# Kernel tuning notes

Measured on AMD Instinct MI355X. Metric: run time of the kernel, lower is better.

The kernel has to match this reference:

```python
import jax, jax.numpy as jnp
import numpy as np

# Problem sizes
N, E, G = 100000, 400000, 2048      # nodes, edges, graphs
NIN, H, NHID, NOUT = 300, 256, 512, 768
NL, T = 3, 16                        # extra atom GAT layers (num_layers=4), pooling timesteps
SLOPE = 0.01                         # leaky_relu negative slope (PyG AttentiveFP uses 0.01)


def setup_inputs() -> dict:
    ks = iter(jax.random.split(jax.random.key(0), 80))
    def rn(shape, s=0.1):
        return jax.random.normal(next(ks), shape, dtype=jnp.float32) * s
    inp = {
        "x": rn((N, NIN), 1.0),
        "edge_attr": rn((E, 1), 1.0),
        # learned parameters (inference mode: dropout disabled)
        "lin1_W": rn((H, NIN)), "lin1_b": rn((H,)),
        # GATEConv
        "g_lin1_W": rn((H, H + 1)), "g_lin2_W": rn((H, H)),
        "g_att_l": rn((H,)), "g_att_r": rn((H,)), "g_bias": rn((H,)),
        "gru0_wih": rn((3 * H, H)), "gru0_whh": rn((3 * H, H)),
        "gru0_bih": rn((3 * H,)), "gru0_bhh": rn((3 * H,)),
        # 3 atom GATConv layers (stacked)
        "atom_W": rn((NL, H, H)), "atom_att_src": rn((NL, H)),
        "atom_att_dst": rn((NL, H)), "atom_bias": rn((NL, H)),
        "agru_wih": rn((NL, 3 * H, H)), "agru_whh": rn((NL, 3 * H, H)),
        "agru_bih": rn((NL, 3 * H)), "agru_bhh": rn((NL, 3 * H)),
        # molecule-level GATConv + GRU (16 timesteps)
        "mol_W": rn((H, H)), "mol_att_src": rn((H,)),
        "mol_att_dst": rn((H,)), "mol_bias": rn((H,)),
        "mgru_wih": rn((3 * H, H)), "mgru_whh": rn((3 * H, H)),
        "mgru_bih": rn((3 * H,)), "mgru_bhh": rn((3 * H,)),
        "lin2_W": rn((NHID, H)), "lin2_b": rn((NHID,)),
        "fc1_W": rn((NOUT, NHID)), "fc1_b": rn((NOUT,)),
        # int inputs
        "edge_index": jax.random.randint(next(ks), (2, E), 0, N),
        "batch": jnp.sort(jax.random.randint(next(ks), (N,), 0, G)),
    }
    return inp


def _lrelu(x):
    return jnp.where(x >= 0, x, SLOPE * x)


def _gru(xin, h, wih, whh, bih, bhh):
    gi = xin @ wih.T + bih
    gh = h @ whh.T + bhh
    ir, iz, inn = jnp.split(gi, 3, axis=-1)
    hr, hz, hn = jnp.split(gh, 3, axis=-1)
    r = jax.nn.sigmoid(ir + hr)
    z = jax.nn.sigmoid(iz + hz)
    n = jnp.tanh(inn + r * hn)
    return (1.0 - z) * n + z * h


def _seg_softmax(a, idx, n):
    m = jax.ops.segment_max(a, idx, num_segments=n)
    e = jnp.exp(a - m[idx])
    s = jax.ops.segment_sum(e, idx, num_segments=n)
    return e / s[idx]


def reference(x, edge_attr, lin1_W, lin1_b, g_lin1_W, g_lin2_W, g_att_l, g_att_r,
              g_bias, gru0_wih, gru0_whh, gru0_bih, gru0_bhh, atom_W, atom_att_src,
              atom_att_dst, atom_bias, agru_wih, agru_whh, agru_bih, agru_bhh,
              mol_W, mol_att_src, mol_att_dst, mol_bias, mgru_wih, mgru_whh,
              mgru_bih, mgru_bhh, lin2_W, lin2_b, fc1_W, fc1_b, edge_index, batch):
    src, dst = edge_index[0], edge_index[1]
    # input projection
    x = _lrelu(x @ lin1_W.T + lin1_b)                                   # [N, H]
    # GATEConv: edge-feature attention
    ge = _lrelu(jnp.concatenate([x[src], edge_attr], axis=-1) @ g_lin1_W.T)  # [E, H]
    a = _lrelu(ge @ g_att_l + (x @ g_att_r)[dst])                       # [E]
    alpha = _seg_softmax(a, dst, N)
    h = jax.ops.segment_sum((x[src] @ g_lin2_W.T) * alpha[:, None], dst,
                            num_segments=N) + g_bias
    x = jax.nn.relu(_gru(jax.nn.elu(h), x, gru0_wih, gru0_whh, gru0_bih, gru0_bhh))
    # remaining atom GATConv + GRU layers
    for l in range(NL):
        xw = x @ atom_W[l].T                                            # [N, H]
        a = _lrelu((xw @ atom_att_src[l])[src] + (xw @ atom_att_dst[l])[dst])
        alpha = _seg_softmax(a, dst, N)
        h = jax.ops.segment_sum(xw[src] * alpha[:, None], dst,
                                num_segments=N) + atom_bias[l]
        x = jax.nn.relu(_gru(jax.nn.elu(h), x, agru_wih[l], agru_whh[l],
                             agru_bih[l], agru_bhh[l]))
    # attentive global pooling (node -> graph bipartite GAT, 16 timesteps)
    out = jax.nn.relu(jax.ops.segment_sum(x, batch, num_segments=G))    # [G, H]
    xw = x @ mol_W.T                                                    # shared lin for src/dst
    a_src = xw @ mol_att_src                                            # [N]
    for _ in range(T):
        a = _lrelu(a_src + ((out @ mol_W.T) @ mol_att_dst)[batch])      # [N]
        alpha = _seg_softmax(a, batch, G)
        h = jax.ops.segment_sum(xw * alpha[:, None], batch,
                                num_segments=G) + mol_bias
        out = jax.nn.relu(_gru(jax.nn.elu(h), out, mgru_wih, mgru_whh,
                               mgru_bih, mgru_bhh))
    out = out @ lin2_W.T + lin2_b                                       # [G, NHID]
    # encoder head: relu -> (global_mean_pool is identity on graph-level emb) -> fc1
    return jax.nn.relu(out) @ fc1_W.T + fc1_b                           # [G, NOUT]
```

## Files before the change

### kernel.cpp

```cpp
#include <hip/hip_runtime.h>
#include <hip/hip_bf16.h>
#include <hip/hip_fp16.h>
#include <math.h>

typedef __attribute__((ext_vector_type(8))) short           short8;
typedef __attribute__((ext_vector_type(8))) unsigned short  ushort8;
typedef __attribute__((ext_vector_type(4))) unsigned short  us4;
typedef __attribute__((ext_vector_type(4))) float           f32x4;

__device__ __forceinline__ float lreluf(float v){ return v >= 0.f ? v : 0.01f*v; }
__device__ __forceinline__ float sigf(float v){ return 1.f/(1.f + expf(-v)); }

#define OP_NONE  0
#define OP_LRELU 1
#define OP_RELU  2

#define GLDS16(gp, lp) __builtin_amdgcn_global_load_lds( \
    (const __attribute__((address_space(1))) void*)(gp), \
    (__attribute__((address_space(3))) void*)(lp), 16, 0, 0)

__device__ __forceinline__ float applyOp(float v, int op){
  if (op == OP_LRELU) return v >= 0.f ? v : 0.01f*v;
  if (op == OP_RELU)  return v > 0.f ? v : 0.f;
  return v;
}

__device__ __forceinline__ unsigned short f2b(float f){
  unsigned x = __float_as_uint(f);
  unsigned lsb = (x >> 16) & 1u;
  return (unsigned short)((x + 0x7fffu + lsb) >> 16);
}
__device__ __forceinline__ float b2f(unsigned short h){
  return __uint_as_float((unsigned)h << 16);
}
__device__ __forceinline__ void split2(float v, unsigned short& h, unsigned short& l){
  h = f2b(v);
  l = f2b(v - b2f(h));
}
__device__ __forceinline__ float rec2(unsigned short h, unsigned short l){
  return b2f(h) + b2f(l);
}
__device__ __forceinline__ unsigned short f2h(float f){
  return __half_as_ushort(__float2half(f));
}
__device__ __forceinline__ float h2f(unsigned short u){
  return __half2float(__ushort_as_half(u));
}

__device__ __forceinline__ int ldsOff(int row, int chunk){
  return row*32 + ((chunk ^ ((row >> 1) & 3)) << 3);
}

__device__ __forceinline__ float blkSum(float v, float* red){
  int t = threadIdx.x;
  red[t] = v; __syncthreads();
  for (int s = 128; s > 0; s >>= 1){ if (t < s) red[t] += red[t+s]; __syncthreads(); }
  float r = red[0]; __syncthreads();
  return r;
}
__device__ __forceinline__ float blkMax(float v, float* red){
  int t = threadIdx.x;
  red[t] = v; __syncthreads();
  for (int s = 128; s > 0; s >>= 1){ if (t < s) red[t] = fmaxf(red[t], red[t+s]); __syncthreads(); }
  float r = red[0]; __syncthreads();
  return r;
}

__device__ __forceinline__ f32x4 mfma3(short8 aH, short8 aL, short8 bH, short8 bL, f32x4 acc){
  acc = __builtin_amdgcn_mfma_f32_16x16x32_bf16(aL, bH, acc, 0, 0, 0);
  acc = __builtin_amdgcn_mfma_f32_16x16x32_bf16(aH, bL, acc, 0, 0, 0);
  acc = __builtin_amdgcn_mfma_f32_16x16x32_bf16(aH, bH, acc, 0, 0, 0);
  return acc;
}

__global__ void wsplit_k(const float* __restrict__ src, unsigned short* __restrict__ Hd,
                         unsigned short* __restrict__ Ld, int lda, int K, long long tot)
{
  long long i = (long long)blockIdx.x*256 + threadIdx.x;
  if (i >= tot) return;
  long long r = i / K; int c = (int)(i % K);
  float v = src[r*lda + c];
  unsigned short h = f2b(v);
  Hd[r*(long long)K + c] = h;
  Ld[r*(long long)K + c] = f2b(v - b2f(h));
}

__device__ __forceinline__ void stagePS(const unsigned short* __restrict__ GH,
    const unsigned short* __restrict__ GL, int ldk, int row0, int k0,
    unsigned short* __restrict__ ldsH, unsigned short* __restrict__ ldsL, int tid)
{
  int r = tid >> 2;
  int c = (tid & 3) ^ ((r >> 1) & 3);
  size_t go = (size_t)(row0 + r)*ldk + k0 + c*8;
  int wbase = (tid >> 6) * 512;
  GLDS16(&GH[go], &ldsH[wbase]);
  GLDS16(&GL[go], &ldsL[wbase]);
}

__device__ __forceinline__ void stage2(const float* __restrict__ src, int lda,
    int row0, int rowmax, int k0, int K,
    unsigned short* __restrict__ ldsH, unsigned short* __restrict__ ldsL, int tid)
{
  int r = tid >> 2, c = tid & 3;
  int gr = row0 + r, gk = k0 + c*8;
  const float* p = src + (size_t)gr*lda + gk;
  float f[8];
  if (gr < rowmax && gk + 8 <= K && ((lda & 3) == 0)){
    float4 f0 = *(const float4*)p;
    float4 f1 = *(const float4*)(p+4);
    f[0]=f0.x; f[1]=f0.y; f[2]=f0.z; f[3]=f0.w;
    f[4]=f1.x; f[5]=f1.y; f[6]=f1.z; f[7]=f1.w;
  } else {
    #pragma unroll
    for (int j = 0; j < 8; ++j) f[j] = (gr < rowmax && gk + j < K) ? p[j] : 0.f;
  }
  ushort8 vh, vl;
  #pragma unroll
  for (int j = 0; j < 8; ++j){
    unsigned short h, l; split2(f[j], h, l);
    vh[j] = h; vl[j] = l;
  }
  int off = ldsOff(r, c);
  *(ushort8*)&ldsH[off] = vh;
  *(ushort8*)&ldsL[off] = vl;
}

__global__ __launch_bounds__(256) void gemm_mfma_k(
    const float* __restrict__ A, int lda,
    const float* __restrict__ W, int ldw,
    const float* __restrict__ bias,
    unsigned short* __restrict__ CH, unsigned short* __restrict__ CL,
    int M, int N, int K, int op)
{
  __shared__ unsigned short AsH[64*32], AsL[64*32];
  __shared__ unsigned short WsH[64*32], WsL[64*32];
  const int tid = threadIdx.x;
  const int bm = blockIdx.y * 64, bn = blockIdx.x * 64;
  const int wave = tid >> 6, lane = tid & 63;
  const int wr = wave >> 1, wc = wave & 1;
  const int quad = lane >> 4, id = lane & 15;

  f32x4 acc[2][2] = {};
  const int iters = (K + 31) / 32;
  for (int kt = 0; kt < iters; ++kt){
    int k0 = kt * 32;
    stage2(A, lda, bm, M, k0, K, AsH, AsL, tid);
    stage2(W, ldw, bn, N, k0, K, WsH, WsL, tid);
    __syncthreads();
    short8 aH[2], aL[2], bH[2], bL[2];
    #pragma unroll
    for (int i = 0; i < 2; ++i){
      int off = ldsOff(wr*32 + i*16 + id, quad);
      aH[i] = *(const short8*)&AsH[off];
      aL[i] = *(const short8*)&AsL[off];
    }
    #pragma unroll
    for (int j = 0; j < 2; ++j){
      int off = ldsOff(wc*32 + j*16 + id, quad);
      bH[j] = *(const short8*)&WsH[off];
      bL[j] = *(const short8*)&WsL[off];
    }
    #pragma unroll
    for (int i = 0; i < 2; ++i)
      #pragma unroll
      for (int j = 0; j < 2; ++j)
        acc[i][j] = mfma3(aH[i], aL[i], bH[j], bL[j], acc[i][j]);
    __syncthreads();
  }
  #pragma unroll
  for (int i = 0; i < 2; ++i){
    int gr0 = bm + wr*32 + i*16 + quad*4;
    #pragma unroll
    for (int j = 0; j < 2; ++j){
      int gc = bn + wc*32 + j*16 + id;
      if (gc >= N) continue;
      float bv = bias ? bias[gc] : 0.f;
      #pragma unroll
      for (int r = 0; r < 4; ++r){
        int row = gr0 + r;
        if (row >= M) continue;
        float v = applyOp(acc[i][j][r] + bv, op);
        unsigned short h, l; split2(v, h, l);
        CH[(size_t)row*N + gc] = h;
        CL[(size_t)row*N + gc] = l;
      }
    }
  }
}

__global__ __launch_bounds__(256) void gemm_ps_k(
    const unsigned short* __restrict__ AH, const unsigned short* __restrict__ AL,
    const unsigned short* __restrict__ WH_, const unsigned short* __restrict__ WL_,
    const float* __restrict__ bias, float* __restrict__ C,
    unsigned short* __restrict__ CH, unsigned short* __restrict__ CL,
    int M, int N, int K, int op, int ncb)
{
  __shared__ unsigned short AsH[64*32], AsL[64*32];
  __shared__ unsigned short WsH[64*32], WsL[64*32];
  int nwg = gridDim.x, bid = blockIdx.x;
  int q = nwg >> 3, r = nwg & 7;
  int xcd = bid & 7, jj = bid >> 3;
  int idx = (xcd < r ? xcd*(q+1) : r*(q+1) + (xcd - r)*q) + jj;
  const int bm = (idx / ncb)*64, bn = (idx % ncb)*64;
  const int tid = threadIdx.x;
  const int wave = tid >> 6, lane = tid & 63;
  const int wr = wave >> 1, wc = wave & 1;
  const int quad = lane >> 4, id = lane & 15;

  f32x4 acc[2][2] = {};
  const int iters = K >> 5;
  for (int kt = 0; kt < iters; ++kt){
    int k0 = kt * 32;
    stagePS(AH, AL, K, bm, k0, AsH, AsL, tid);
    stagePS(WH_, WL_, K, bn, k0, WsH, WsL, tid);
    __syncthreads();
    short8 aH[2], aL[2], bH[2], bL[2];
    #pragma unroll
    for (int i = 0; i < 2; ++i){
      int off = ldsOff(wr*32 + i*16 + id, quad);
      aH[i] = *(const short8*)&AsH[off];
      aL[i] = *(const short8*)&AsL[off];
    }
    #pragma unroll
    for (int j = 0; j < 2; ++j){
      int off = ldsOff(wc*32 + j*16 + id, quad);
      bH[j] = *(const short8*)&WsH[off];
      bL[j] = *(const short8*)&WsL[off];
    }
    #pragma unroll
    for (int i = 0; i < 2; ++i)
      #pragma unroll
      for (int j = 0; j < 2; ++j)
        acc[i][j] = mfma3(aH[i], aL[i], bH[j], bL[j], acc[i][j]);
    __syncthreads();
  }
  #pragma unroll
  for (int i = 0; i < 2; ++i){
    int gr0 = bm + wr*32 + i*16 + quad*4;
    #pragma unroll
    for (int j = 0; j < 2; ++j){
      int gc = bn + wc*32 + j*16 + id;
      float bv = bias ? bias[gc] : 0.f;
      #pragma unroll
      for (int rr = 0; rr < 4; ++rr){
        int row = gr0 + rr;
        if (row >= M) continue;
        float v = applyOp(acc[i][j][rr] + bv, op);
        if (C)  C[(size_t)row*N + gc] = v;
        if (CH){
          if (CL){
            unsigned short h, l; split2(v, h, l);
            CH[(size_t)row*N + gc] = h;
            CL[(size_t)row*N + gc] = l;
          } else {
            CH[(size_t)row*N + gc] = f2h(v);
          }
        }
      }
    }
  }
}

__global__ __launch_bounds__(256) void gemm2_ps_k(
    const unsigned short* __restrict__ AH, const unsigned short* __restrict__ AL,
    const unsigned short* __restrict__ W1H, const unsigned short* __restrict__ W1L,
    const unsigned short* __restrict__ W2H, const unsigned short* __restrict__ W2L,
    unsigned short* __restrict__ YB, unsigned short* __restrict__ ZB, int M)
{
  __shared__ unsigned short AsH[64*32], AsL[64*32];
  __shared__ unsigned short U1H[64*32], U1L[64*32];
  __shared__ unsigned short U2H[64*32], U2L[64*32];
  int nwg = gridDim.x, bid = blockIdx.x;
  int q = nwg >> 3, r = nwg & 7;
  int xcd = bid & 7, jj = bid >> 3;
  int idx = (xcd < r ? xcd*(q+1) : r*(q+1) + (xcd - r)*q) + jj;
  const int bm = (idx >> 2)*64, bn = (idx & 3)*64;
  const int tid = threadIdx.x;
  const int wave = tid >> 6, lane = tid & 63;
  const int wr = wave >> 1, wc = wave & 1;
  const int quad = lane >> 4, id = lane & 15;

  f32x4 acc1[2][2] = {}, acc2[2][2] = {};
  for (int kt = 0; kt < 8; ++kt){
    int k0 = kt * 32;
    stagePS(AH, AL, 256, bm, k0, AsH, AsL, tid);
    stagePS(W1H, W1L, 256, bn, k0, U1H, U1L, tid);
    stagePS(W2H, W2L, 256, bn, k0, U2H, U2L, tid);
    __syncthreads();
    short8 aH[2], aL[2];
    #pragma unroll
    for (int i = 0; i < 2; ++i){
      int off = ldsOff(wr*32 + i*16 + id, quad);
      aH[i] = *(const short8*)&AsH[off];
      aL[i] = *(const short8*)&AsL[off];
    }
    #pragma unroll
    for (int j = 0; j < 2; ++j){
      int off = ldsOff(wc*32 + j*16 + id, quad);
      short8 bh, bl;
      bh = *(const short8*)&U1H[off]; bl = *(const short8*)&U1L[off];
      #pragma unroll
      for (int i = 0; i < 2; ++i) acc1[i][j] = mfma3(aH[i], aL[i], bh, bl, acc1[i][j]);
      bh = *(const short8*)&U2H[off]; bl = *(const short8*)&U2L[off];
      #pragma unroll
      for (int i = 0; i < 2; ++i) acc2[i][j] = mfma3(aH[i], aL[i], bh, bl, acc2[i][j]);
    }
    __syncthreads();
  }
  #pragma unroll
  for (int i = 0; i < 2; ++i){
    int gr0 = bm + wr*32 + i*16 + quad*4;
    #pragma unroll
    for (int j = 0; j < 2; ++j){
      int gc = bn + wc*32 + j*16 + id;
      #pragma unroll
      for (int rr = 0; rr < 4; ++rr){
        int row = gr0 + rr;
        if (row >= M) continue;
        YB[(size_t)row*256 + gc] = f2h(acc1[i][j][rr]);
        ZB[(size_t)row*256 + gc] = f2h(acc2[i][j][rr]);
      }
    }
  }
}

__device__ __forceinline__ void gru_phase_ps(
    const unsigned short* __restrict__ AH, const unsigned short* __restrict__ AL,
    const unsigned short* __restrict__ WH_, const unsigned short* __restrict__ WL_,
    int bm, int bn, int tid, int wr, int wc, int quad, int id,
    unsigned short* AsH, unsigned short* AsL,
    unsigned short* W0H, unsigned short* W0L,
    unsigned short* W1H, unsigned short* W1L,
    unsigned short* W2H, unsigned short* W2L,
    f32x4 (&accR)[2][2], f32x4 (&accZ)[2][2], f32x4 (&accN)[2][2])
{
  for (int kt = 0; kt < 8; ++kt){
    int k0 = kt * 32;
    stagePS(AH, AL, 256, bm, k0, AsH, AsL, tid);
    stagePS(WH_,          WL_,          256, bn, k0, W0H, W0L, tid);
    stagePS(WH_ + 65536,  WL_ + 65536,  256, bn, k0, W1H, W1L, tid);
    stagePS(WH_ + 131072, WL_ + 131072, 256, bn, k0, W2H, W2L, tid);
    __syncthreads();
    short8 aH[2], aL[2];
    #pragma unroll
    for (int i = 0; i < 2; ++i){
      int off = ldsOff(wr*32 + i*16 + id, quad);
      aH[i] = *(const short8*)&AsH[off];
      aL[i] = *(const short8*)&AsL[off];
    }
    #pragma unroll
    for (int j = 0; j < 2; ++j){
      int off = ldsOff(wc*32 + j*16 + id, quad);
      short8 bh, bl;
      bh = *(const short8*)&W0H[off]; bl = *(const short8*)&W0L[off];
      #pragma unroll
      for (int i = 0; i < 2; ++i) accR[i][j] = mfma3(aH[i], aL[i], bh, bl, accR[i][j]);
      bh = *(const short8*)&W1H[off]; bl = *(const short8*)&W1L[off];
      #pragma unroll
      for (int i = 0; i < 2; ++i) accZ[i][j] = mfma3(aH[i], aL[i], bh, bl, accZ[i][j]);
      bh = *(const short8*)&W2H[off]; bl = *(const short8*)&W2L[off];
      #pragma unroll
      for (int i = 0; i < 2; ++i) accN[i][j] = mfma3(aH[i], aL[i], bh, bl, accN[i][j]);
    }
    __syncthreads();
  }
}

__global__ __launch_bounds__(256) void gru_ps_k(
    const unsigned short* __restrict__ XinH, const unsigned short* __restrict__ XinL,
    const unsigned short* __restrict__ HidH, const unsigned short* __restrict__ HidL,
    const unsigned short* __restrict__ wihH, const unsigned short* __restrict__ wihL,
    const unsigned short* __restrict__ whhH, const unsigned short* __restrict__ whhL,
    const float* __restrict__ bih, const float* __restrict__ bhh,
    unsigned short* __restrict__ OutH, unsigned short* __restrict__ OutL, int M)
{
  __shared__ unsigned short AsH[64*32], AsL[64*32];
  __shared__ unsigned short W0H[64*32], W0L[64*32];
  __shared__ unsigned short W1H[64*32], W1L[64*32];
  __shared__ unsigned short W2H[64*32], W2L[64*32];
  int nwg = gridDim.x, bid = blockIdx.x;
  int q = nwg >> 3, r = nwg & 7;
  int xcd = bid & 7, jj = bid >> 3;
  int idx = (xcd < r ? xcd*(q+1) : r*(q+1) + (xcd - r)*q) + jj;
  const int bm = (idx >> 2)*64, bn = (idx & 3)*64;
  const int tid = threadIdx.x;
  const int wave = tid >> 6, lane = tid & 63;
  const int wr = wave >> 1, wc = wave & 1;
  const int quad = lane >> 4, id = lane & 15;

  f32x4 accR[2][2] = {}, accZ[2][2] = {}, accI[2][2] = {}, accH[2][2] = {};

  gru_phase_ps(XinH, XinL, wihH, wihL, bm, bn, tid, wr, wc, quad, id,
               AsH, AsL, W0H, W0L, W1H, W1L, W2H, W2L, accR, accZ, accI);
  gru_phase_ps(HidH, HidL, whhH, whhL, bm, bn, tid, wr, wc, quad, id,
               AsH, AsL, W0H, W0L, W1H, W1L, W2H, W2L, accR, accZ, accH);

  #pragma unroll
  for (int i = 0; i < 2; ++i){
    int gr0 = bm + wr*32 + i*16 + quad*4;
    #pragma unroll
    for (int j = 0; j < 2; ++j){
      int gc = bn + wc*32 + j*16 + id;
      float br_  = bih[gc]     + bhh[gc];
      float bz_  = bih[256+gc] + bhh[256+gc];
      float bn_i = bih[512+gc], bn_h = bhh[512+gc];
      #pragma unroll
      for (int rr = 0; rr < 4; ++rr){
        int row = gr0 + rr;
        if (row >= M) continue;
        float rg = sigf(accR[i][j][rr] + br_);
        float zg = sigf(accZ[i][j][rr] + bz_);
        float ng = tanhf(accI[i][j][rr] + bn_i + rg*(accH[i][j][rr] + bn_h));
        float hv = rec2(HidH[(size_t)row*256 + gc], HidL[(size_t)row*256 + gc]);
        float o = (1.f - zg)*ng + zg*hv;
        o = o > 0.f ? o : 0.f;
        unsigned short h, l; split2(o, h, l);
        OutH[(size_t)row*256 + gc] = h;
        OutL[(size_t)row*256 + gc] = l;
      }
    }
  }
}

__global__ __launch_bounds__(256) void rowdot2_ps_k(
    const unsigned short* __restrict__ XH, const unsigned short* __restrict__ XL,
    const float* __restrict__ w1, const float* __restrict__ w2,
    float* __restrict__ y1, float* __restrict__ y2, int M)
{
  int m = blockIdx.x*4 + (threadIdx.x >> 6);
  if (m >= M) return;
  int lane = threadIdx.x & 63;
  us4 vh = *(const us4*)&XH[(size_t)m*256 + lane*4];
  us4 vl = *(const us4*)&XL[(size_t)m*256 + lane*4];
  float p1 = 0.f, p2 = 0.f;
  #pragma unroll
  for (int u = 0; u < 4; ++u){
    float xv = rec2(vh[u], vl[u]);
    int c = lane*4 + u;
    p1 += xv * w1[c];
    if (w2) p2 += xv * w2[c];
  }
  for (int o = 32; o > 0; o >>= 1){
    p1 += __shfl_down(p1, o);
    if (w2) p2 += __shfl_down(p2, o);
  }
  if (lane == 0){ y1[m] = p1; if (w2) y2[m] = p2; }
}

__global__ __launch_bounds__(256) void rowdot_b_k(
    const unsigned short* __restrict__ XB,
    const float* __restrict__ w1, const float* __restrict__ w2,
    float* __restrict__ y1, float* __restrict__ y2, int M)
{
  int m = blockIdx.x*4 + (threadIdx.x >> 6);
  if (m >= M) return;
  int lane = threadIdx.x & 63;
  us4 vh = *(const us4*)&XB[(size_t)m*256 + lane*4];
  float p1 = 0.f, p2 = 0.f;
  #pragma unroll
  for (int u = 0; u < 4; ++u){
    float xv = h2f(vh[u]);
    int c = lane*4 + u;
    p1 += xv * w1[c];
    if (w2) p2 += xv * w2[c];
  }
  for (int o = 32; o > 0; o >>= 1){
    p1 += __shfl_down(p1, o);
    if (w2) p2 += __shfl_down(p2, o);
  }
  if (lane == 0){ y1[m] = p1; if (w2) y2[m] = p2; }
}

__global__ void hist_k(const int* __restrict__ key, unsigned* __restrict__ deg, int E){
  int e = blockIdx.x*256 + threadIdx.x;
  if (e >= E) return;
  atomicAdd(&deg[key[e]], 1u);
}

__global__ __launch_bounds__(256) void scan1_k(const unsigned* __restrict__ deg,
    unsigned* __restrict__ incl, unsigned* __restrict__ bsum, int N)
{
  __shared__ unsigned sm[256];
  int t = threadIdx.x;
  int i = blockIdx.x*256 + t;
  unsigned v = (i < N) ? deg[i] : 0u;
  sm[t] = v; __syncthreads();
  for (int s = 1; s < 256; s <<= 1){
    unsigned u = (t >= s) ? sm[t - s] : 0u;
    __syncthreads();
    sm[t] += u;
    __syncthreads();
  }
  if (i < N) incl[i] = sm[t];
  if (t == 255) bsum[blockIdx.x] = sm[255];
}

__global__ __launch_bounds__(256) void scan2_k(unsigned* __restrict__ bsum, int nb){
  __shared__ unsigned sm[256];
  __shared__ unsigned carry;
  int t = threadIdx.x;
  if (t == 0) carry = 0u;
  __syncthreads();
  for (int base = 0; base < nb; base += 256){
    int i = base + t;
    unsigned v = (i < nb) ? bsum[i] : 0u;
    sm[t] = v; __syncthreads();
    for (int s = 1; s < 256; s <<= 1){
      unsigned u = (t >= s) ? sm[t - s] : 0u;
      __syncthreads();
      sm[t] += u;
      __syncthreads();
    }
    unsigned total = sm[255];
    unsigned c = carry;
    if (i < nb) bsum[i] = c + sm[t] - v;
    __syncthreads();
    if (t == 0) carry = c + total;
    __syncthreads();
  }
}

__global__ void scan3_k(const unsigned* __restrict__ incl, const unsigned* __restrict__ deg,
    const unsigned* __restrict__ bsum, unsigned* __restrict__ off, int N, int E)
{
  int i = blockIdx.x*256 + threadIdx.x;
  if (i < N) off[i] = incl[i] - deg[i] + bsum[blockIdx.x];
  if (i == 0) off[N] = (unsigned)E;
}

__global__ void fill_k(const int* __restrict__ src, const int* __restrict__ dst,
    const unsigned* __restrict__ off, unsigned* __restrict__ cur,
    int* __restrict__ csr_src, int* __restrict__ csr_eid, int* __restrict__ epos, int E)
{
  int e = blockIdx.x*256 + threadIdx.x;
  if (e >= E) return;
  int d = dst[e];
  unsigned p = off[d] + atomicAdd(&cur[d], 1u);
  csr_src[p] = src[e];
  csr_eid[p] = e;
  epos[e] = (int)p;
}

__global__ void fill2_k(const int* __restrict__ src, const int* __restrict__ epos,
    const unsigned* __restrict__ off2, unsigned* __restrict__ cur,
    int* __restrict__ csc_pos, int E)
{
  int e = blockIdx.x*256 + threadIdx.x;
  if (e >= E) return;
  int s = src[e];
  unsigned qq = off2[s] + atomicAdd(&cur[s], 1u);
  csc_pos[qq] = epos[e];
}

__global__ __launch_bounds__(256) void gate_edge_score_csc_k(
    const unsigned short* __restrict__ YB,
    const float* __restrict__ g_lin1W,
    const float* __restrict__ att_l, const float* __restrict__ ea_in,
    const float* __restrict__ xr,
    const unsigned* __restrict__ off2, const int* __restrict__ csc_pos,
    const int* __restrict__ csr_eid, const int* __restrict__ dst,
    float* __restrict__ a_out, int N, int H)
{
  int s = blockIdx.x*4 + (threadIdx.x >> 6);
  if (s >= N) return;
  int lane = threadIdx.x & 63;
  unsigned q0 = off2[s], q1 = off2[s+1];
  if (q0 == q1) return;
  us4 vh = *(const us4*)&YB[(size_t)s*256 + lane*4];
  float y4[4], w4[4], a4[4];
  #pragma unroll
  for (int u = 0; u < 4; ++u){
    int c = lane*4 + u;
    y4[u] = h2f(vh[u]);
    w4[u] = g_lin1W[(size_t)c*(H+1) + H];
    a4[u] = att_l[c];
  }
  for (unsigned qq = q0; qq < q1; ++qq){
    int p = csc_pos[qq];
    int e = csr_eid[p];
    int d = dst[e];
    float eav = ea_in[e];
    float acc = 0.f;
    #pragma unroll
    for (int u = 0; u < 4; ++u)
      acc += lreluf(y4[u] + eav * w4[u]) * a4[u];
    for (int o = 32; o > 0; o >>= 1) acc += __shfl_down(acc, o);
    if (lane == 0) a_out[p] = lreluf(acc + xr[d]);
  }
}

__global__ void node_softmax_k(const unsigned* __restrict__ off, const int* __restrict__ csr_src,
    const float* __restrict__ nd1, const float* __restrict__ nd2,
    float* __restrict__ w, int N, int mode)
{
  int n = blockIdx.x*256 + threadIdx.x;
  if (n >= N) return;
  unsigned p0 = off[n], p1 = off[n+1];
  float m = -INFINITY;
  if (mode){
    float d = nd2[n];
    for (unsigned p = p0; p < p1; ++p){
      float a = lreluf(nd1[csr_src[p]] + d);
      w[p] = a;
      m = fmaxf(m, a);
    }
  } else {
    for (unsigned p = p0; p < p1; ++p) m = fmaxf(m, w[p]);
  }
  float ssum = 0.f;
  for (unsigned p = p0; p < p1; ++p){
    float e = expf(w[p] - m);
    w[p] = e; ssum += e;
  }
  float inv = (ssum > 0.f) ? 1.f/ssum : 0.f;
  for (unsigned p = p0; p < p1; ++p) w[p] *= inv;
}

__global__ __launch_bounds__(256) void gather_h_k(
    const unsigned short* __restrict__ ZB,
    const float* __restrict__ w, const unsigned* __restrict__ off,
    const int* __restrict__ csr_src, const float* __restrict__ bias,
    unsigned short* __restrict__ hH, unsigned short* __restrict__ hL, int N)
{
  int n = blockIdx.x*4 + (threadIdx.x >> 6);
  if (n >= N) return;
  int lane = threadIdx.x & 63;
  unsigned p0 = off[n], p1 = off[n+1];
  float4 acc = make_float4(0.f, 0.f, 0.f, 0.f);
  if (p0 < p1){
    us4 zh_n = *(const us4*)&ZB[(size_t)csr_src[p0]*256 + lane*4];
    float w_n = w[p0];
    for (unsigned p = p0; p < p1; ++p){
      us4 zh = zh_n;
      float wv = w_n;
      if (p + 1 < p1){
        zh_n = *(const us4*)&ZB[(size_t)csr_src[p+1]*256 + lane*4];
        w_n = w[p+1];
      }
      acc.x = fmaf(wv, h2f(zh[0]), acc.x);
      acc.y = fmaf(wv, h2f(zh[1]), acc.y);
      acc.z = fmaf(wv, h2f(zh[2]), acc.z);
      acc.w = fmaf(wv, h2f(zh[3]), acc.w);
    }
  }
  const float4 b = *(const float4*)&bias[lane*4];
  float vals[4];
  float v;
  v = acc.x + b.x; vals[0] = v > 0.f ? v : expf(v) - 1.f;
  v = acc.y + b.y; vals[1] = v > 0.f ? v : expf(v) - 1.f;
  v = acc.z + b.z; vals[2] = v > 0.f ? v : expf(v) - 1.f;
  v = acc.w + b.w; vals[3] = v > 0.f ? v : expf(v) - 1.f;
  us4 vh, vl;
  #pragma unroll
  for (int u = 0; u < 4; ++u){
    unsigned short h, l; split2(vals[u], h, l);
    vh[u] = h; vl[u] = l;
  }
  *(us4*)&hH[(size_t)n*256 + lane*4] = vh;
  *(us4*)&hL[(size_t)n*256 + lane*4] = vl;
}

__global__ void seg_bounds_k(const int* __restrict__ batch, unsigned* __restrict__ gs,
                             unsigned* __restrict__ ge, int N){
  int n = blockIdx.x*256 + threadIdx.x;
  if (n >= N) return;
  int g = batch[n];
  atomicMin(&gs[g], (unsigned)n);
  atomicMax(&ge[g], (unsigned)(n+1));
}
__global__ __launch_bounds__(256) void graph_pool_k(
    const unsigned short* __restrict__ xH, const unsigned short* __restrict__ xL,
    const unsigned* __restrict__ gs, const unsigned* __restrict__ ge,
    unsigned short* __restrict__ outgH, unsigned short* __restrict__ outgL)
{
  int g = blockIdx.x, t = threadIdx.x;
  unsigned s0 = gs[g], e0 = ge[g];
  float acc = 0.f;
  for (unsigned n = s0; n < e0; ++n)
    acc += rec2(xH[(size_t)n*256 + t], xL[(size_t)n*256 + t]);
  acc = acc > 0.f ? acc : 0.f;
  unsigned short h, l; split2(acc, h, l);
  outgH[(size_t)g*256 + t] = h;
  outgL[(size_t)g*256 + t] = l;
}
__global__ void precompute_v_k(const float* __restrict__ W, const float* __restrict__ ad,
                               float* __restrict__ v){
  int i = threadIdx.x;
  float acc = 0.f;
  for (int j = 0; j < 256; ++j) acc += W[(size_t)j*256 + i] * ad[j];
  v[i] = acc;
}
__global__ __launch_bounds__(256) void mol_pool_k(
    const unsigned short* __restrict__ ogH, const unsigned short* __restrict__ ogL,
    const float* __restrict__ v, const float* __restrict__ asrc,
    const unsigned short* __restrict__ xwB,
    const unsigned* __restrict__ gs, const unsigned* __restrict__ geb,
    const float* __restrict__ bias,
    unsigned short* __restrict__ hgH, unsigned short* __restrict__ hgL)
{
  __shared__ float red[256];
  int g = blockIdx.x, t = threadIdx.x;
  float ogv = rec2(ogH[(size_t)g*256 + t], ogL[(size_t)g*256 + t]);
  float tg = blkSum(ogv * v[t], red);
  unsigned s0 = gs[g], e0 = geb[g];
  float mx = -INFINITY;
  for (unsigned n = s0 + t; n < e0; n += 256) mx = fmaxf(mx, lreluf(asrc[n] + tg));
  mx = blkMax(mx, red);
  float sm = 0.f;
  for (unsigned n = s0 + t; n < e0; n += 256) sm += expf(lreluf(asrc[n] + tg) - mx);
  sm = blkSum(sm, red);
  float acc = 0.f;
  if (e0 > s0 && sm > 0.f){
    float inv = 1.f / sm;
    for (unsigned n = s0; n < e0; ++n){
      float w = expf(lreluf(asrc[n] + tg) - mx) * inv;
      acc = fmaf(w, h2f(xwB[(size_t)n*256 + t]), acc);
    }
  }
  float h0 = acc + bias[t];
  h0 = h0 > 0.f ? h0 : expf(h0) - 1.f;
  unsigned short h, l; split2(h0, h, l);
  hgH[(size_t)g*256 + t] = h;
  hgL[(size_t)g*256 + t] = l;
}

extern "C" void kernel_launch(void* const* d_in, const int* in_sizes, int n_in,
                              void* d_out, int out_size, void* d_ws, size_t ws_size,
                              hipStream_t stream)
{
  (void)n_in; (void)ws_size;
  const int H    = in_sizes[3];
  const int NIN  = in_sizes[2] / H;
  const int N    = in_sizes[0] / NIN;
  const int E    = in_sizes[1];
  const int NL   = in_sizes[16] / H;
  const int NHID = in_sizes[30];
  const int NOUT = in_sizes[32];
  const int G    = out_size / NOUT;
  const int T    = 16;

  const float* x_in     = (const float*)d_in[0];
  const float* ea_in    = (const float*)d_in[1];
  const float* lin1_W   = (const float*)d_in[2];
  const float* lin1_b   = (const float*)d_in[3];
  const float* g_lin1W  = (const float*)d_in[4];
  const float* g_lin2W  = (const float*)d_in[5];
  const float* g_att_l  = (const float*)d_in[6];
  const float* g_att_r  = (const float*)d_in[7];
  const float* g_bias   = (const float*)d_in[8];
  const float* gru0_wih = (const float*)d_in[9];
  const float* gru0_whh = (const float*)d_in[10];
  const float* gru0_bih = (const float*)d_in[11];
  const float* gru0_bhh = (const float*)d_in[12];
  const float* atom_W   = (const float*)d_in[13];
  const float* atom_as  = (const float*)d_in[14];
  const float* atom_ad  = (const float*)d_in[15];
  const float* atom_b   = (const float*)d_in[16];
  const float* agru_wih = (const float*)d_in[17];
  const float* agru_whh = (const float*)d_in[18];
  const float* agru_bih = (const float*)d_in[19];
  const float* agru_bhh = (const float*)d_in[20];
  const float* mol_W    = (const float*)d_in[21];
  const float* mol_as   = (const float*)d_in[22];
  const float* mol_ad   = (const float*)d_in[23];
  const float* mol_b    = (const float*)d_in[24];
  const float* mgru_wih = (const float*)d_in[25];
  const float* mgru_whh = (const float*)d_in[26];
  const float* mgru_bih = (const float*)d_in[27];
  const float* mgru_bhh = (const float*)d_in[28];
  const float* lin2_W   = (const float*)d_in[29];
  const float* lin2_b   = (const float*)d_in[30];
  const float* fc1_W    = (const float*)d_in[31];
  const float* fc1_b    = (const float*)d_in[32];
  const int*  eidx      = (const int*)d_in[33];
  const int*  batch     = (const int*)d_in[34];
  const int*  srcI = eidx;
  const int*  dstI = eidx + E;

  char* wp = (char*)d_ws;
  auto alloc = [&](size_t bytes)->void*{
    void* p = (void*)wp;
    wp += (bytes + 255) & ~(size_t)255;
    return p;
  };
  auto allocUS = [&](size_t elems)->unsigned short*{ return (unsigned short*)alloc(elems*2); };

  unsigned short *xH   = allocUS((size_t)N*H), *xL   = allocUS((size_t)N*H);
  unsigned short *hbH  = allocUS((size_t)N*H), *hbL  = allocUS((size_t)N*H);
  unsigned short *outH = allocUS((size_t)N*H), *outL = allocUS((size_t)N*H);
  unsigned short *xwB  = allocUS((size_t)N*H);
  float*    ea    = (float*)alloc((size_t)E*4);
  float*    nd1   = (float*)alloc((size_t)N*4);
  float*    nd2   = (float*)alloc((size_t)N*4);
  unsigned short *ogH  = allocUS((size_t)G*H), *ogL  = allocUS((size_t)G*H);
  unsigned short *og2H = allocUS((size_t)G*H), *og2L = allocUS((size_t)G*H);
  unsigned short *hgH  = allocUS((size_t)G*H), *hgL  = allocUS((size_t)G*H);
  unsigned short *o2H  = allocUS((size_t)G*NHID), *o2L = allocUS((size_t)G*NHID);
  unsigned* gsb   = (unsigned*)alloc((size_t)G*4);
  unsigned* geb   = (unsigned*)alloc((size_t)G*4);
  float*    vvec  = (float*)alloc((size_t)H*4);
  const int nb = (N + 255) / 256;
  unsigned* deg     = (unsigned*)alloc((size_t)N*4);
  unsigned* cur     = (unsigned*)alloc((size_t)N*4);
  unsigned* incl    = (unsigned*)alloc((size_t)N*4);
  unsigned* off     = (unsigned*)alloc((size_t)(N+1)*4);
  unsigned* off2    = (unsigned*)alloc((size_t)(N+1)*4);
  unsigned* bsum    = (unsigned*)alloc((size_t)nb*4);
  int*      csr_src = (int*)alloc((size_t)E*4);
  int*      csr_eid = (int*)alloc((size_t)E*4);
  int*      epos    = (int*)alloc((size_t)E*4);
  int*      csc_pos = (int*)alloc((size_t)E*4);
  const size_t WG = (size_t)768*256;
  const size_t WS = (size_t)256*256;
  unsigned short *g0ihH = allocUS(WG), *g0ihL = allocUS(WG);
  unsigned short *g0hhH = allocUS(WG), *g0hhL = allocUS(WG);
  unsigned short *aihH  = allocUS(WG*NL), *aihL = allocUS(WG*NL);
  unsigned short *ahhH  = allocUS(WG*NL), *ahhL = allocUS(WG*NL);
  unsigned short *mihH  = allocUS(WG), *mihL = allocUS(WG);
  unsigned short *mhhH  = allocUS(WG), *mhhL = allocUS(WG);
  unsigned short *gl1H  = allocUS(WS), *gl1L = allocUS(WS);
  unsigned short *gl2H  = allocUS(WS), *gl2L = allocUS(WS);
  unsigned short *atWH  = allocUS(WS*NL), *atWL = allocUS(WS*NL);
  unsigned short *molH  = allocUS(WS), *molL = allocUS(WS);
  unsigned short *l2WH  = allocUS((size_t)NHID*256), *l2WL = allocUS((size_t)NHID*256);
  unsigned short *f1WH  = allocUS((size_t)NOUT*NHID), *f1WL = allocUS((size_t)NOUT*NHID);

  auto gemmps = [&](const unsigned short* AH_, const unsigned short* AL_,
                    const unsigned short* WH_, const unsigned short* WL_,
                    const float* bias, float* C, unsigned short* CH, unsigned short* CL,
                    int M_, int N_, int K_, int op){
    int ncb = N_ / 64;
    int nwg = ((M_ + 63)/64) * ncb;
    gemm_ps_k<<<dim3(nwg), dim3(256), 0, stream>>>(AH_, AL_, WH_, WL_, bias, C, CH, CL,
                                                   M_, N_, K_, op, ncb);
  };
  auto grup = [&](const unsigned short* XiH, const unsigned short* XiL,
                  const unsigned short* HiH, const unsigned short* HiL,
                  const unsigned short* ihH, const unsigned short* ihL,
                  const unsigned short* hhH, const unsigned short* hhL,
                  const float* bih, const float* bhh,
                  unsigned short* OH, unsigned short* OL, int M_){
    int nwg = ((M_ + 63)/64)*4;
    gru_ps_k<<<dim3(nwg), dim3(256), 0, stream>>>(XiH, XiL, HiH, HiL,
                                                  ihH, ihL, hhH, hhL, bih, bhh,
                                                  OH, OL, M_);
  };
  auto wsplit = [&](const float* src, unsigned short* Hd, unsigned short* Ld,
                    int lda, int K, long long rows){
    long long tot = rows * K;
    wsplit_k<<<dim3((unsigned)((tot + 255)/256)), dim3(256), 0, stream>>>(src, Hd, Ld, lda, K, tot);
  };

  wsplit(gru0_wih, g0ihH, g0ihL, 256, 256, 768);
  wsplit(gru0_whh, g0hhH, g0hhL, 256, 256, 768);
  wsplit(agru_wih, aihH, aihL, 256, 256, (long long)NL*768);
  wsplit(agru_whh, ahhH, ahhL, 256, 256, (long long)NL*768);
  wsplit(mgru_wih, mihH, mihL, 256, 256, 768);
  wsplit(mgru_whh, mhhH, mhhL, 256, 256, 768);
  wsplit(g_lin1W,  gl1H, gl1L, H+1, 256, 256);
  wsplit(g_lin2W,  gl2H, gl2L, 256, 256, 256);
  wsplit(atom_W,   atWH, atWL, 256, 256, (long long)NL*256);
  wsplit(mol_W,    molH, molL, 256, 256, 256);
  wsplit(lin2_W,   l2WH, l2WL, 256, 256, NHID);
  wsplit(fc1_W,    f1WH, f1WL, NHID, NHID, NOUT);

  hipMemsetAsync(deg, 0, (size_t)N*4, stream);
  hist_k<<<dim3((E+255)/256), dim3(256), 0, stream>>>(dstI, deg, E);
  scan1_k<<<dim3(nb), dim3(256), 0, stream>>>(deg, incl, bsum, N);
  scan2_k<<<dim3(1), dim3(256), 0, stream>>>(bsum, nb);
  scan3_k<<<dim3(nb), dim3(256), 0, stream>>>(incl, deg, bsum, off, N, E);
  hipMemsetAsync(cur, 0, (size_t)N*4, stream);
  fill_k<<<dim3((E+255)/256), dim3(256), 0, stream>>>(srcI, dstI, off, cur, csr_src, csr_eid, epos, E);
  hipMemsetAsync(deg, 0, (size_t)N*4, stream);
  hist_k<<<dim3((E+255)/256), dim3(256), 0, stream>>>(srcI, deg, E);
  scan1_k<<<dim3(nb), dim3(256), 0, stream>>>(deg, incl, bsum, N);
  scan2_k<<<dim3(1), dim3(256), 0, stream>>>(bsum, nb);
  scan3_k<<<dim3(nb), dim3(256), 0, stream>>>(incl, deg, bsum, off2, N, E);
  hipMemsetAsync(cur, 0, (size_t)N*4, stream);
  fill2_k<<<dim3((E+255)/256), dim3(256), 0, stream>>>(srcI, epos, off2, cur, csc_pos, E);

  {
    dim3 gr(4, (N + 63)/64);
    gemm_mfma_k<<<gr, dim3(256), 0, stream>>>(x_in, NIN, lin1_W, NIN, lin1_b,
                                              xH, xL, N, H, NIN, OP_LRELU);
  }

  {
    int nwg = ((N + 63)/64)*4;
    gemm2_ps_k<<<dim3(nwg), dim3(256), 0, stream>>>(xH, xL, gl1H, gl1L, gl2H, gl2L,
                                                    outH, xwB, N);
  }
  rowdot2_ps_k<<<dim3((N+3)/4), dim3(256), 0, stream>>>(xH, xL, g_att_r, (const float*)nullptr,
                                                        nd1, (float*)nullptr, N);
  gate_edge_score_csc_k<<<dim3((N+3)/4), dim3(256), 0, stream>>>(outH, g_lin1W, g_att_l,
                                                                 ea_in, nd1, off2, csc_pos,
                                                                 csr_eid, dstI, ea, N, H);
  node_softmax_k<<<dim3(nb), dim3(256), 0, stream>>>(off, csr_src, nullptr, nullptr, ea, N, 0);
  gather_h_k<<<dim3((N+3)/4), dim3(256), 0, stream>>>(xwB, ea, off, csr_src, g_bias,
                                                      hbH, hbL, N);
  grup(hbH, hbL, xH, xL, g0ihH, g0ihL, g0hhH, g0hhL, gru0_bih, gru0_bhh, outH, outL, N);
  { unsigned short* t = xH; xH = outH; outH = t; t = xL; xL = outL; outL = t; }

  for (int l = 0; l < NL; ++l){
    gemmps(xH, xL, atWH + (size_t)l*WS, atWL + (size_t)l*WS, nullptr,
           nullptr, xwB, nullptr, N, 256, 256, OP_NONE);
    rowdot_b_k<<<dim3((N+3)/4), dim3(256), 0, stream>>>(xwB, atom_as + (size_t)l*H,
                                                        atom_ad + (size_t)l*H, nd1, nd2, N);
    node_softmax_k<<<dim3(nb), dim3(256), 0, stream>>>(off, csr_src, nd1, nd2, ea, N, 1);
    gather_h_k<<<dim3((N+3)/4), dim3(256), 0, stream>>>(xwB, ea, off, csr_src,
                                                        atom_b + (size_t)l*H, hbH, hbL, N);
    grup(hbH, hbL, xH, xL,
         aihH + (size_t)l*WG, aihL + (size_t)l*WG,
         ahhH + (size_t)l*WG, ahhL + (size_t)l*WG,
         agru_bih + (size_t)l*3*H, agru_bhh + (size_t)l*3*H, outH, outL, N);
    { unsigned short* t = xH; xH = outH; outH = t; t = xL; xL = outL; outL = t; }
  }

  hipMemsetAsync(gsb, 0xFF, (size_t)G*4, stream);
  hipMemsetAsync(geb, 0x00, (size_t)G*4, stream);
  seg_bounds_k<<<dim3((N+255)/256), dim3(256), 0, stream>>>(batch, gsb, geb, N);
  graph_pool_k<<<dim3(G), dim3(256), 0, stream>>>(xH, xL, gsb, geb, ogH, ogL);
  gemmps(xH, xL, molH, molL, nullptr, nullptr, xwB, nullptr, N, 256, 256, OP_NONE);
  rowdot_b_k<<<dim3((N+3)/4), dim3(256), 0, stream>>>(xwB, mol_as, (const float*)nullptr,
                                                      nd1, (float*)nullptr, N);
  precompute_v_k<<<dim3(1), dim3(256), 0, stream>>>(mol_W, mol_ad, vvec);
  unsigned short *cogH = ogH, *cogL = ogL, *cog2H = og2H, *cog2L = og2L;
  for (int t = 0; t < T; ++t){
    mol_pool_k<<<dim3(G), dim3(256), 0, stream>>>(cogH, cogL, vvec, nd1, xwB,
                                                  gsb, geb, mol_b, hgH, hgL);
    grup(hgH, hgL, cogH, cogL, mihH, mihL, mhhH, mhhL, mgru_bih, mgru_bhh,
         cog2H, cog2L, G);
    { unsigned short* tt = cogH; cogH = cog2H; cog2H = tt;
      tt = cogL; cogL = cog2L; cog2L = tt; }
  }

  gemmps(cogH, cogL, l2WH, l2WL, lin2_b, nullptr, o2H, o2L, G, NHID, 256, OP_RELU);
  gemmps(o2H, o2L, f1WH, f1WL, fc1_b, (float*)d_out, nullptr, nullptr, G, NOUT, NHID, OP_NONE);
}
```

Baseline: 3.656 ms.

## Store node activations as single fp16 and use fp16 MFMA with split weights

Replaces the bf16 hi/lo split representation of node activations with a single fp16 buffer. The node-level GEMMs and GRUs now issue two fp16 MFMAs per tile (activation times weight-hi and weight-lo) instead of three bf16 MFMAs. This halves activation memory traffic and LDS staging and cuts MFMA count. The graph-level path keeps split activations, which preserves accuracy there. The cost is lower activation precision, since fp16 has a reduced range and no lo term, which risks accuracy drift across the layers.

```diff
diff --git a/kernel.cpp b/kernel.cpp
--- a/kernel.cpp
+++ b/kernel.cpp
@@ -1,9 +1,7 @@
 #include <hip/hip_runtime.h>
-#include <hip/hip_bf16.h>
-#include <hip/hip_fp16.h>
 #include <math.h>
 
-typedef __attribute__((ext_vector_type(8))) short           short8;
+typedef __attribute__((ext_vector_type(8))) _Float16        half8;
 typedef __attribute__((ext_vector_type(8))) unsigned short  ushort8;
 typedef __attribute__((ext_vector_type(4))) unsigned short  us4;
 typedef __attribute__((ext_vector_type(4))) float           f32x4;
@@ -25,30 +23,27 @@
   return v;
 }
 
-__device__ __forceinline__ unsigned short f2b(float f){
-  unsigned x = __float_as_uint(f);
-  unsigned lsb = (x >> 16) & 1u;
-  return (unsigned short)((x + 0x7fffu + lsb) >> 16);
-}
-__device__ __forceinline__ float b2f(unsigned short h){
-  return __uint_as_float((unsigned)h << 16);
-}
-__device__ __forceinline__ void split2(float v, unsigned short& h, unsigned short& l){
-  h = f2b(v);
-  l = f2b(v - b2f(h));
-}
-__device__ __forceinline__ float rec2(unsigned short h, unsigned short l){
-  return b2f(h) + b2f(l);
-}
 __device__ __forceinline__ unsigned short f2h(float f){
-  return __half_as_ushort(__float2half(f));
+  _Float16 h = (_Float16)f;
+  return *(unsigned short*)&h;
 }
 __device__ __forceinline__ float h2f(unsigned short u){
-  return __half2float(__ushort_as_half(u));
-}
-
-__device__ __forceinline__ int ldsOff(int row, int chunk){
+  _Float16 h = *(_Float16*)&u;
+  return (float)h;
+}
+__device__ __forceinline__ void split2h(float v, unsigned short& h, unsigned short& l){
+  h = f2h(v);
+  l = f2h(v - h2f(h));
+}
+__device__ __forceinline__ float rec2h(unsigned short h, unsigned short l){
+  return h2f(h) + h2f(l);
+}
+
+__device__ __forceinline__ int ldsOff32(int row, int chunk){
   return row*32 + ((chunk ^ ((row >> 1) & 3)) << 3);
+}
+__device__ __forceinline__ int ldsOff64(int row, int chunk){
+  return row*64 + ((chunk ^ ((row >> 1) & 7)) << 3);
 }
 
 __device__ __forceinline__ float blkSum(float v, float* red){
@@ -66,38 +61,47 @@
   return r;
 }
 
-__device__ __forceinline__ f32x4 mfma3(short8 aH, short8 aL, short8 bH, short8 bL, f32x4 acc){
-  acc = __builtin_amdgcn_mfma_f32_16x16x32_bf16(aL, bH, acc, 0, 0, 0);
-  acc = __builtin_amdgcn_mfma_f32_16x16x32_bf16(aH, bL, acc, 0, 0, 0);
-  acc = __builtin_amdgcn_mfma_f32_16x16x32_bf16(aH, bH, acc, 0, 0, 0);
-  return acc;
-}
-
-__global__ void wsplit_k(const float* __restrict__ src, unsigned short* __restrict__ Hd,
-                         unsigned short* __restrict__ Ld, int lda, int K, long long tot)
+__device__ __forceinline__ f32x4 mfma16(half8 a, half8 b, f32x4 acc){
+  return __builtin_amdgcn_mfma_f32_16x16x32_f16(a, b, acc, 0, 0, 0);
+}
+
+__global__ void wsplit16_k(const float* __restrict__ src, unsigned short* __restrict__ Hd,
+                           unsigned short* __restrict__ Ld, int lda, int K, long long tot)
 {
   long long i = (long long)blockIdx.x*256 + threadIdx.x;
   if (i >= tot) return;
   long long r = i / K; int c = (int)(i % K);
   float v = src[r*lda + c];
-  unsigned short h = f2b(v);
+  unsigned short h, l; split2h(v, h, l);
   Hd[r*(long long)K + c] = h;
-  Ld[r*(long long)K + c] = f2b(v - b2f(h));
-}
-
-__device__ __forceinline__ void stagePS(const unsigned short* __restrict__ GH,
-    const unsigned short* __restrict__ GL, int ldk, int row0, int k0,
-    unsigned short* __restrict__ ldsH, unsigned short* __restrict__ ldsL, int tid)
+  Ld[r*(long long)K + c] = l;
+}
+
+__device__ __forceinline__ void stage16b(const unsigned short* __restrict__ G,
+    int ldk, int row0, int rowmax, int k0, unsigned short* __restrict__ lds, int tid)
 {
   int r = tid >> 2;
+  int gr = row0 + r; if (gr >= rowmax) gr = rowmax - 1;
   int c = (tid & 3) ^ ((r >> 1) & 3);
-  size_t go = (size_t)(row0 + r)*ldk + k0 + c*8;
+  size_t go = (size_t)gr*ldk + k0 + c*8;
   int wbase = (tid >> 6) * 512;
-  GLDS16(&GH[go], &ldsH[wbase]);
-  GLDS16(&GL[go], &ldsL[wbase]);
-}
-
-__device__ __forceinline__ void stage2(const float* __restrict__ src, int lda,
+  GLDS16(&G[go], &lds[wbase]);
+}
+__device__ __forceinline__ void stage16(const unsigned short* __restrict__ G,
+    int ldk, int row0, int rowmax, int k0, unsigned short* __restrict__ lds, int tid)
+{
+  #pragma unroll
+  for (int p = 0; p < 2; ++p){
+    int r = p*32 + (tid >> 3);
+    int gr = row0 + r; if (gr >= rowmax) gr = rowmax - 1;
+    int c = (tid & 7) ^ ((r >> 1) & 7);
+    size_t go = (size_t)gr*ldk + k0 + c*8;
+    int wbase = p*2048 + (tid >> 6)*512;
+    GLDS16(&G[go], &lds[wbase]);
+  }
+}
+
+__device__ __forceinline__ void stage_f32s(const float* __restrict__ src, int lda,
     int row0, int rowmax, int k0, int K,
     unsigned short* __restrict__ ldsH, unsigned short* __restrict__ ldsL, int tid)
 {
@@ -117,23 +121,23 @@
   ushort8 vh, vl;
   #pragma unroll
   for (int j = 0; j < 8; ++j){
-    unsigned short h, l; split2(f[j], h, l);
+    unsigned short h, l; split2h(f[j], h, l);
     vh[j] = h; vl[j] = l;
   }
-  int off = ldsOff(r, c);
+  int off = ldsOff32(r, c);
   *(ushort8*)&ldsH[off] = vh;
   *(ushort8*)&ldsL[off] = vl;
 }
 
-__global__ __launch_bounds__(256) void gemm_mfma_k(
+__global__ __launch_bounds__(256) void gemm_l1_k(
     const float* __restrict__ A, int lda,
     const float* __restrict__ W, int ldw,
     const float* __restrict__ bias,
-    unsigned short* __restrict__ CH, unsigned short* __restrict__ CL,
+    unsigned short* __restrict__ CB,
     int M, int N, int K, int op)
 {
-  __shared__ unsigned short AsH[64*32], AsL[64*32];
-  __shared__ unsigned short WsH[64*32], WsL[64*32];
+  __shared__ unsigned short AsH[2048], AsL[2048];
+  __shared__ unsigned short WsH[2048], WsL[2048];
   const int tid = threadIdx.x;
   const int bm = blockIdx.y * 64, bn = blockIdx.x * 64;
   const int wave = tid >> 6, lane = tid & 63;
@@ -144,27 +148,30 @@
   const int iters = (K + 31) / 32;
   for (int kt = 0; kt < iters; ++kt){
     int k0 = kt * 32;
-    stage2(A, lda, bm, M, k0, K, AsH, AsL, tid);
-    stage2(W, ldw, bn, N, k0, K, WsH, WsL, tid);
-    __syncthreads();
-    short8 aH[2], aL[2], bH[2], bL[2];
+    stage_f32s(A, lda, bm, M, k0, K, AsH, AsL, tid);
+    stage_f32s(W, ldw, bn, N, k0, K, WsH, WsL, tid);
+    __syncthreads();
+    half8 aH[2], aL[2], bH[2], bL[2];
     #pragma unroll
     for (int i = 0; i < 2; ++i){
-      int off = ldsOff(wr*32 + i*16 + id, quad);
-      aH[i] = *(const short8*)&AsH[off];
-      aL[i] = *(const short8*)&AsL[off];
+      int off = ldsOff32(wr*32 + i*16 + id, quad);
+      aH[i] = *(const half8*)&AsH[off];
+      aL[i] = *(const half8*)&AsL[off];
     }
     #pragma unroll
     for (int j = 0; j < 2; ++j){
-      int off = ldsOff(wc*32 + j*16 + id, quad);
-      bH[j] = *(const short8*)&WsH[off];
-      bL[j] = *(const short8*)&WsL[off];
+      int off = ldsOff32(wc*32 + j*16 + id, quad);
+      bH[j] = *(const half8*)&WsH[off];
+      bL[j] = *(const half8*)&WsL[off];
     }
     #pragma unroll
     for (int i = 0; i < 2; ++i)
       #pragma unroll
-      for (int j = 0; j < 2; ++j)
-        acc[i][j] = mfma3(aH[i], aL[i], bH[j], bL[j], acc[i][j]);
+      for (int j = 0; j < 2; ++j){
+        acc[i][j] = mfma16(aH[i], bH[j], acc[i][j]);
+        acc[i][j] = mfma16(aL[i], bH[j], acc[i][j]);
+        acc[i][j] = mfma16(aH[i], bL[j], acc[i][j]);
+      }
     __syncthreads();
   }
   #pragma unroll
@@ -179,24 +186,354 @@
       for (int r = 0; r < 4; ++r){
         int row = gr0 + r;
         if (row >= M) continue;
-        float v = applyOp(acc[i][j][r] + bv, op);
-        unsigned short h, l; split2(v, h, l);
-        CH[(size_t)row*N + gc] = h;
-        CL[(size_t)row*N + gc] = l;
-      }
-    }
-  }
-}
-
-__global__ __launch_bounds__(256) void gemm_ps_k(
+        CB[(size_t)row*N + gc] = f2h(applyOp(acc[i][j][r] + bv, op));
+      }
+    }
+  }
+}
+
+__global__ __launch_bounds__(256) void gemm16s_k(
+    const unsigned short* __restrict__ A,
+    const unsigned short* __restrict__ WH_, const unsigned short* __restrict__ WL_,
+    unsigned short* __restrict__ CB, int M)
+{
+  __shared__ unsigned short As[2048];
+  __shared__ unsigned short WsH[2048], WsL[2048];
+  int nwg = gridDim.x, bid = blockIdx.x;
+  int q = nwg >> 3, r = nwg & 7;
+  int xcd = bid & 7, jj = bid >> 3;
+  int idx = (xcd < r ? xcd*(q+1) : r*(q+1) + (xcd - r)*q) + jj;
+  const int bm = (idx >> 2)*64, bn = (idx & 3)*64;
+  const int tid = threadIdx.x;
+  const int wave = tid >> 6, lane = tid & 63;
+  const int wr = wave >> 1, wc = wave & 1;
+  const int quad = lane >> 4, id = lane & 15;
+
+  f32x4 acc[2][2] = {};
+  for (int kt = 0; kt < 8; ++kt){
+    int k0 = kt * 32;
+    stage16b(A, 256, bm, M, k0, As, tid);
+    stage16b(WH_, 256, bn, 256, k0, WsH, tid);
+    stage16b(WL_, 256, bn, 256, k0, WsL, tid);
+    __syncthreads();
+    half8 a[2];
+    #pragma unroll
+    for (int i = 0; i < 2; ++i)
+      a[i] = *(const half8*)&As[ldsOff32(wr*32 + i*16 + id, quad)];
+    #pragma unroll
+    for (int j = 0; j < 2; ++j){
+      int off = ldsOff32(wc*32 + j*16 + id, quad);
+      half8 bh = *(const half8*)&WsH[off];
+      half8 bl = *(const half8*)&WsL[off];
+      #pragma unroll
+      for (int i = 0; i < 2; ++i){
+        acc[i][j] = mfma16(a[i], bh, acc[i][j]);
+        acc[i][j] = mfma16(a[i], bl, acc[i][j]);
+      }
+    }
+    __syncthreads();
+  }
+  #pragma unroll
+  for (int i = 0; i < 2; ++i){
+    int gr0 = bm + wr*32 + i*16 + quad*4;
+    #pragma unroll
+    for (int j = 0; j < 2; ++j){
+      int gc = bn + wc*32 + j*16 + id;
+      #pragma unroll
+      for (int rr = 0; rr < 4; ++rr){
+        int row = gr0 + rr;
+        if (row < M) CB[(size_t)row*256 + gc] = f2h(acc[i][j][rr]);
+      }
+    }
+  }
+}
+
+__global__ __launch_bounds__(256) void gemm2s_k(
+    const unsigned short* __restrict__ A,
+    const unsigned short* __restrict__ W1H, const unsigned short* __restrict__ W1L,
+    const unsigned short* __restrict__ W2H, const unsigned short* __restrict__ W2L,
+    unsigned short* __restrict__ YB, unsigned short* __restrict__ ZB, int M)
+{
+  __shared__ unsigned short As[2048];
+  __shared__ unsigned short U1H[2048], U1L[2048], U2H[2048], U2L[2048];
+  int nwg = gridDim.x, bid = blockIdx.x;
+  int q = nwg >> 3, r = nwg & 7;
+  int xcd = bid & 7, jj = bid >> 3;
+  int idx = (xcd < r ? xcd*(q+1) : r*(q+1) + (xcd - r)*q) + jj;
+  const int bm = (idx >> 2)*64, bn = (idx & 3)*64;
+  const int tid = threadIdx.x;
+  const int wave = tid >> 6, lane = tid & 63;
+  const int wr = wave >> 1, wc = wave & 1;
+  const int quad = lane >> 4, id = lane & 15;
+
+  f32x4 acc1[2][2] = {}, acc2[2][2] = {};
+  for (int kt = 0; kt < 8; ++kt){
+    int k0 = kt * 32;
+    stage16b(A, 256, bm, M, k0, As, tid);
+    stage16b(W1H, 256, bn, 256, k0, U1H, tid);
+    stage16b(W1L, 256, bn, 256, k0, U1L, tid);
+    stage16b(W2H, 256, bn, 256, k0, U2H, tid);
+    stage16b(W2L, 256, bn, 256, k0, U2L, tid);
+    __syncthreads();
+    half8 a[2];
+    #pragma unroll
+    for (int i = 0; i < 2; ++i)
+      a[i] = *(const half8*)&As[ldsOff32(wr*32 + i*16 + id, quad)];
+    #pragma unroll
+    for (int j = 0; j < 2; ++j){
+      int off = ldsOff32(wc*32 + j*16 + id, quad);
+      half8 b1h = *(const half8*)&U1H[off];
+      half8 b1l = *(const half8*)&U1L[off];
+      half8 b2h = *(const half8*)&U2H[off];
+      half8 b2l = *(const half8*)&U2L[off];
+      #pragma unroll
+      for (int i = 0; i < 2; ++i){
+        acc1[i][j] = mfma16(a[i], b1h, acc1[i][j]);
+        acc1[i][j] = mfma16(a[i], b1l, acc1[i][j]);
+        acc2[i][j] = mfma16(a[i], b2h, acc2[i][j]);
+        acc2[i][j] = mfma16(a[i], b2l, acc2[i][j]);
+      }
+    }
+    __syncthreads();
+  }
+  #pragma unroll
+  for (int i = 0; i < 2; ++i){
+    int gr0 = bm + wr*32 + i*16 + quad*4;
+    #pragma unroll
+    for (int j = 0; j < 2; ++j){
+      int gc = bn + wc*32 + j*16 + id;
+      #pragma unroll
+      for (int rr = 0; rr < 4; ++rr){
+        int row = gr0 + rr;
+        if (row >= M) continue;
+        YB[(size_t)row*256 + gc] = f2h(acc1[i][j][rr]);
+        ZB[(size_t)row*256 + gc] = f2h(acc2[i][j][rr]);
+      }
+    }
+  }
+}
+
+__device__ __forceinline__ void gru_phase_s(
+    const unsigned short* __restrict__ A,
+    const unsigned short* __restrict__ WH, const unsigned short* __restrict__ WL,
+    int M, int bm, int bn, int tid, int wr, int wc, int quad, int id,
+    unsigned short* As,
+    unsigned short* W0H, unsigned short* W0L,
+    unsigned short* W1H, unsigned short* W1L,
+    unsigned short* W2H, unsigned short* W2L,
+    f32x4 (&accR)[2][2], f32x4 (&accZ)[2][2], f32x4 (&accN)[2][2])
+{
+  for (int kt = 0; kt < 8; ++kt){
+    int k0 = kt * 32;
+    stage16b(A, 256, bm, M, k0, As, tid);
+    stage16b(WH,          256, bn, 256, k0, W0H, tid);
+    stage16b(WL,          256, bn, 256, k0, W0L, tid);
+    stage16b(WH + 65536,  256, bn, 256, k0, W1H, tid);
+    stage16b(WL + 65536,  256, bn, 256, k0, W1L, tid);
+    stage16b(WH + 131072, 256, bn, 256, k0, W2H, tid);
+    stage16b(WL + 131072, 256, bn, 256, k0, W2L, tid);
+    __syncthreads();
+    half8 a[2];
+    #pragma unroll
+    for (int i = 0; i < 2; ++i)
+      a[i] = *(const half8*)&As[ldsOff32(wr*32 + i*16 + id, quad)];
+    #pragma unroll
+    for (int j = 0; j < 2; ++j){
+      int off = ldsOff32(wc*32 + j*16 + id, quad);
+      half8 bh, bl;
+      bh = *(const half8*)&W0H[off]; bl = *(const half8*)&W0L[off];
+      #pragma unroll
+      for (int i = 0; i < 2; ++i){
+        accR[i][j] = mfma16(a[i], bh, accR[i][j]);
+        accR[i][j] = mfma16(a[i], bl, accR[i][j]);
+      }
+      bh = *(const half8*)&W1H[off]; bl = *(const half8*)&W1L[off];
+      #pragma unroll
+      for (int i = 0; i < 2; ++i){
+        accZ[i][j] = mfma16(a[i], bh, accZ[i][j]);
+        accZ[i][j] = mfma16(a[i], bl, accZ[i][j]);
+      }
+      bh = *(const half8*)&W2H[off]; bl = *(const half8*)&W2L[off];
+      #pragma unroll
+      for (int i = 0; i < 2; ++i){
+        accN[i][j] = mfma16(a[i], bh, accN[i][j]);
+        accN[i][j] = mfma16(a[i], bl, accN[i][j]);
+      }
+    }
+    __syncthreads();
+  }
+}
+
+__global__ __launch_bounds__(256) void gru16_k(
+    const unsigned short* __restrict__ Xin, const unsigned short* __restrict__ Hid,
+    const unsigned short* __restrict__ wihH, const unsigned short* __restrict__ wihL,
+    const unsigned short* __restrict__ whhH, const unsigned short* __restrict__ whhL,
+    const float* __restrict__ bih, const float* __restrict__ bhh,
+    unsigned short* __restrict__ Out, int M)
+{
+  __shared__ unsigned short As[2048];
+  __shared__ unsigned short W0H[2048], W0L[2048];
+  __shared__ unsigned short W1H[2048], W1L[2048];
+  __shared__ unsigned short W2H[2048], W2L[2048];
+  int nwg = gridDim.x, bid = blockIdx.x;
+  int q = nwg >> 3, r = nwg & 7;
+  int xcd = bid & 7, jj = bid >> 3;
+  int idx = (xcd < r ? xcd*(q+1) : r*(q+1) + (xcd - r)*q) + jj;
+  const int bm = (idx >> 2)*64, bn = (idx & 3)*64;
+  const int tid = threadIdx.x;
+  const int wave = tid >> 6, lane = tid & 63;
+  const int wr = wave >> 1, wc = wave & 1;
+  const int quad = lane >> 4, id = lane & 15;
+
+  f32x4 accR[2][2] = {}, accZ[2][2] = {}, accI[2][2] = {}, accH[2][2] = {};
+
+  gru_phase_s(Xin, wihH, wihL, M, bm, bn, tid, wr, wc, quad, id,
+              As, W0H, W0L, W1H, W1L, W2H, W2L, accR, accZ, accI);
+  gru_phase_s(Hid, whhH, whhL, M, bm, bn, tid, wr, wc, quad, id,
+              As, W0H, W0L, W1H, W1L, W2H, W2L, accR, accZ, accH);
+
+  #pragma unroll
+  for (int i = 0; i < 2; ++i){
+    int gr0 = bm + wr*32 + i*16 + quad*4;
+    #pragma unroll
+    for (int j = 0; j < 2; ++j){
+      int gc = bn + wc*32 + j*16 + id;
+      float br_  = bih[gc]     + bhh[gc];
+      float bz_  = bih[256+gc] + bhh[256+gc];
+      float bn_i = bih[512+gc], bn_h = bhh[512+gc];
+      #pragma unroll
+      for (int rr = 0; rr < 4; ++rr){
+        int row = gr0 + rr;
+        if (row >= M) continue;
+        float rg = sigf(accR[i][j][rr] + br_);
+        float zg = sigf(accZ[i][j][rr] + bz_);
+        float ng = tanhf(accI[i][j][rr] + bn_i + rg*(accH[i][j][rr] + bn_h));
+        float hv = h2f(Hid[(size_t)row*256 + gc]);
+        float o = (1.f - zg)*ng + zg*hv;
+        o = o > 0.f ? o : 0.f;
+        Out[(size_t)row*256 + gc] = f2h(o);
+      }
+    }
+  }
+}
+
+__device__ __forceinline__ void gru_phase16m(
+    const unsigned short* __restrict__ AH, const unsigned short* __restrict__ AL,
+    const unsigned short* __restrict__ WH, const unsigned short* __restrict__ WL,
+    int M, int bm, int bn, int tid, int wr, int wc, int quad, int id,
+    unsigned short* AsH, unsigned short* AsL,
+    unsigned short* W0, unsigned short* W1, unsigned short* W2,
+    unsigned short* W0L, unsigned short* W1L, unsigned short* W2L,
+    f32x4 (&accR)[2][2], f32x4 (&accZ)[2][2], f32x4 (&accN)[2][2])
+{
+  for (int kt = 0; kt < 8; ++kt){
+    int k0 = kt * 32;
+    stage16b(AH, 256, bm, M, k0, AsH, tid);
+    stage16b(AL, 256, bm, M, k0, AsL, tid);
+    stage16b(WH,          256, bn, 256, k0, W0,  tid);
+    stage16b(WH + 65536,  256, bn, 256, k0, W1,  tid);
+    stage16b(WH + 131072, 256, bn, 256, k0, W2,  tid);
+    stage16b(WL,          256, bn, 256, k0, W0L, tid);
+    stage16b(WL + 65536,  256, bn, 256, k0, W1L, tid);
+    stage16b(WL + 131072, 256, bn, 256, k0, W2L, tid);
+    __syncthreads();
+    half8 aH[2], aL[2];
+    #pragma unroll
+    for (int i = 0; i < 2; ++i){
+      int off = ldsOff32(wr*32 + i*16 + id, quad);
+      aH[i] = *(const half8*)&AsH[off];
+      aL[i] = *(const half8*)&AsL[off];
+    }
+    #pragma unroll
+    for (int j = 0; j < 2; ++j){
+      int off = ldsOff32(wc*32 + j*16 + id, quad);
+      half8 bh, bl;
+      bh = *(const half8*)&W0[off]; bl = *(const half8*)&W0L[off];
+      #pragma unroll
+      for (int i = 0; i < 2; ++i){
+        accR[i][j] = mfma16(aH[i], bh, accR[i][j]);
+        accR[i][j] = mfma16(aL[i], bh, accR[i][j]);
+        accR[i][j] = mfma16(aH[i], bl, accR[i][j]);
+      }
+      bh = *(const half8*)&W1[off]; bl = *(const half8*)&W1L[off];
+      #pragma unroll
+      for (int i = 0; i < 2; ++i){
+        accZ[i][j] = mfma16(aH[i], bh, accZ[i][j]);
+        accZ[i][j] = mfma16(aL[i], bh, accZ[i][j]);
+        accZ[i][j] = mfma16(aH[i], bl, accZ[i][j]);
+      }
+      bh = *(const half8*)&W2[off]; bl = *(const half8*)&W2L[off];
+      #pragma unroll
+      for (int i = 0; i < 2; ++i){
+        accN[i][j] = mfma16(aH[i], bh, accN[i][j]);
+        accN[i][j] = mfma16(aL[i], bh, accN[i][j]);
+        accN[i][j] = mfma16(aH[i], bl, accN[i][j]);
+      }
+    }
+    __syncthreads();
+  }
+}
+
+__global__ __launch_bounds__(256) void gru16m_k(
+    const unsigned short* __restrict__ XinH, const unsigned short* __restrict__ XinL,
+    const unsigned short* __restrict__ HidH, const unsigned short* __restrict__ HidL,
+    const unsigned short* __restrict__ wihH, const unsigned short* __restrict__ wihL,
+    const unsigned short* __restrict__ whhH, const unsigned short* __restrict__ whhL,
+    const float* __restrict__ bih, const float* __restrict__ bhh,
+    unsigned short* __restrict__ OutH, unsigned short* __restrict__ OutL, int M)
+{
+  __shared__ unsigned short AsH[2048], AsL[2048];
+  __shared__ unsigned short W0[2048], W1[2048], W2[2048];
+  __shared__ unsigned short W0L[2048], W1L[2048], W2L[2048];
+  const int bm = (blockIdx.x >> 2)*64, bn = (blockIdx.x & 3)*64;
+  const int tid = threadIdx.x;
+  const int wave = tid >> 6, lane = tid & 63;
+  const int wr = wave >> 1, wc = wave & 1;
+  const int quad = lane >> 4, id = lane & 15;
+
+  f32x4 accR[2][2] = {}, accZ[2][2] = {}, accI[2][2] = {}, accH[2][2] = {};
+
+  gru_phase16m(XinH, XinL, wihH, wihL, M, bm, bn, tid, wr, wc, quad, id,
+               AsH, AsL, W0, W1, W2, W0L, W1L, W2L, accR, accZ, accI);
+  gru_phase16m(HidH, HidL, whhH, whhL, M, bm, bn, tid, wr, wc, quad, id,
+               AsH, AsL, W0, W1, W2, W0L, W1L, W2L, accR, accZ, accH);
+
+  #pragma unroll
+  for (int i = 0; i < 2; ++i){
+    int gr0 = bm + wr*32 + i*16 + quad*4;
+    #pragma unroll
+    for (int j = 0; j < 2; ++j){
+      int gc = bn + wc*32 + j*16 + id;
+      float br_  = bih[gc]     + bhh[gc];
+      float bz_  = bih[256+gc] + bhh[256+gc];
+      float bn_i = bih[512+gc], bn_h = bhh[512+gc];
+      #pragma unroll
+      for (int rr = 0; rr < 4; ++rr){
+        int row = gr0 + rr;
+        if (row >= M) continue;
+        float rg = sigf(accR[i][j][rr] + br_);
+        float zg = sigf(accZ[i][j][rr] + bz_);
+        float ng = tanhf(accI[i][j][rr] + bn_i + rg*(accH[i][j][rr] + bn_h));
+        float hv = rec2h(HidH[(size_t)row*256 + gc], HidL[(size_t)row*256 + gc]);
+        float o = (1.f - zg)*ng + zg*hv;
+        o = o > 0.f ? o : 0.f;
+        unsigned short h, l; split2h(o, h, l);
+        OutH[(size_t)row*256 + gc] = h;
+        OutL[(size_t)row*256 + gc] = l;
+      }
+    }
+  }
+}
+
+__global__ __launch_bounds__(256) void gemm16p_k(
     const unsigned short* __restrict__ AH, const unsigned short* __restrict__ AL,
     const unsigned short* __restrict__ WH_, const unsigned short* __restrict__ WL_,
     const float* __restrict__ bias, float* __restrict__ C,
     unsigned short* __restrict__ CH, unsigned short* __restrict__ CL,
     int M, int N, int K, int op, int ncb)
 {
-  __shared__ unsigned short AsH[64*32], AsL[64*32];
-  __shared__ unsigned short WsH[64*32], WsL[64*32];
+  __shared__ unsigned short AsH[4096], AsL[4096];
+  __shared__ unsigned short Ws[4096], WsL[4096];
   int nwg = gridDim.x, bid = blockIdx.x;
   int q = nwg >> 3, r = nwg & 7;
   int xcd = bid & 7, jj = bid >> 3;
@@ -208,30 +545,37 @@
   const int quad = lane >> 4, id = lane & 15;
 
   f32x4 acc[2][2] = {};
-  const int iters = K >> 5;
+  const int iters = K >> 6;
   for (int kt = 0; kt < iters; ++kt){
-    int k0 = kt * 32;
-    stagePS(AH, AL, K, bm, k0, AsH, AsL, tid);
-    stagePS(WH_, WL_, K, bn, k0, WsH, WsL, tid);
-    __syncthreads();
-    short8 aH[2], aL[2], bH[2], bL[2];
-    #pragma unroll
-    for (int i = 0; i < 2; ++i){
-      int off = ldsOff(wr*32 + i*16 + id, quad);
-      aH[i] = *(const short8*)&AsH[off];
-      aL[i] = *(const short8*)&AsL[off];
-    }
-    #pragma unroll
-    for (int j = 0; j < 2; ++j){
-      int off = ldsOff(wc*32 + j*16 + id, quad);
-      bH[j] = *(const short8*)&WsH[off];
-      bL[j] = *(const short8*)&WsL[off];
-    }
-    #pragma unroll
-    for (int i = 0; i < 2; ++i)
-      #pragma unroll
-      for (int j = 0; j < 2; ++j)
-        acc[i][j] = mfma3(aH[i], aL[i], bH[j], bL[j], acc[i][j]);
+    int k0 = kt * 64;
+    stage16(AH, K, bm, M, k0, AsH, tid);
+    stage16(AL, K, bm, M, k0, AsL, tid);
+    stage16(WH_, K, bn, N, k0, Ws, tid);
+    stage16(WL_, K, bn, N, k0, WsL, tid);
+    __syncthreads();
+    #pragma unroll
+    for (int kh = 0; kh < 2; ++kh){
+      int ch = kh*4 + quad;
+      half8 aH[2], aL[2];
+      #pragma unroll
+      for (int i = 0; i < 2; ++i){
+        int off = ldsOff64(wr*32 + i*16 + id, ch);
+        aH[i] = *(const half8*)&AsH[off];
+        aL[i] = *(const half8*)&AsL[off];
+      }
+      #pragma unroll
+      for (int j = 0; j < 2; ++j){
+        int off = ldsOff64(wc*32 + j*16 + id, ch);
+        half8 b = *(const half8*)&Ws[off];
+        half8 bl = *(const half8*)&WsL[off];
+        #pragma unroll
+        for (int i = 0; i < 2; ++i){
+          acc[i][j] = mfma16(aH[i], b, acc[i][j]);
+          acc[i][j] = mfma16(aL[i], b, acc[i][j]);
+          acc[i][j] = mfma16(aH[i], bl, acc[i][j]);
+        }
+      }
+    }
     __syncthreads();
   }
   #pragma unroll
@@ -248,206 +592,16 @@
         float v = applyOp(acc[i][j][rr] + bv, op);
         if (C)  C[(size_t)row*N + gc] = v;
         if (CH){
-          if (CL){
-            unsigned short h, l; split2(v, h, l);
-            CH[(size_t)row*N + gc] = h;
-            CL[(size_t)row*N + gc] = l;
-          } else {
-            CH[(size_t)row*N + gc] = f2h(v);
-          }
+          unsigned short h, l; split2h(v, h, l);
+          CH[(size_t)row*N + gc] = h;
+          CL[(size_t)row*N + gc] = l;
         }
       }
     }
   }
 }
 
-__global__ __launch_bounds__(256) void gemm2_ps_k(
-    const unsigned short* __restrict__ AH, const unsigned short* __restrict__ AL,
-    const unsigned short* __restrict__ W1H, const unsigned short* __restrict__ W1L,
-    const unsigned short* __restrict__ W2H, const unsigned short* __restrict__ W2L,
-    unsigned short* __restrict__ YB, unsigned short* __restrict__ ZB, int M)
-{
-  __shared__ unsigned short AsH[64*32], AsL[64*32];
-  __shared__ unsigned short U1H[64*32], U1L[64*32];
-  __shared__ unsigned short U2H[64*32], U2L[64*32];
-  int nwg = gridDim.x, bid = blockIdx.x;
-  int q = nwg >> 3, r = nwg & 7;
-  int xcd = bid & 7, jj = bid >> 3;
-  int idx = (xcd < r ? xcd*(q+1) : r*(q+1) + (xcd - r)*q) + jj;
-  const int bm = (idx >> 2)*64, bn = (idx & 3)*64;
-  const int tid = threadIdx.x;
-  const int wave = tid >> 6, lane = tid & 63;
-  const int wr = wave >> 1, wc = wave & 1;
-  const int quad = lane >> 4, id = lane & 15;
-
-  f32x4 acc1[2][2] = {}, acc2[2][2] = {};
-  for (int kt = 0; kt < 8; ++kt){
-    int k0 = kt * 32;
-    stagePS(AH, AL, 256, bm, k0, AsH, AsL, tid);
-    stagePS(W1H, W1L, 256, bn, k0, U1H, U1L, tid);
-    stagePS(W2H, W2L, 256, bn, k0, U2H, U2L, tid);
-    __syncthreads();
-    short8 aH[2], aL[2];
-    #pragma unroll
-    for (int i = 0; i < 2; ++i){
-      int off = ldsOff(wr*32 + i*16 + id, quad);
-      aH[i] = *(const short8*)&AsH[off];
-      aL[i] = *(const short8*)&AsL[off];
-    }
-    #pragma unroll
-    for (int j = 0; j < 2; ++j){
-      int off = ldsOff(wc*32 + j*16 + id, quad);
-      short8 bh, bl;
-      bh = *(const short8*)&U1H[off]; bl = *(const short8*)&U1L[off];
-      #pragma unroll
-      for (int i = 0; i < 2; ++i) acc1[i][j] = mfma3(aH[i], aL[i], bh, bl, acc1[i][j]);
-      bh = *(const short8*)&U2H[off]; bl = *(const short8*)&U2L[off];
-      #pragma unroll
-      for (int i = 0; i < 2; ++i) acc2[i][j] = mfma3(aH[i], aL[i], bh, bl, acc2[i][j]);
-    }
-    __syncthreads();
-  }
-  #pragma unroll
-  for (int i = 0; i < 2; ++i){
-    int gr0 = bm + wr*32 + i*16 + quad*4;
-    #pragma unroll
-    for (int j = 0; j < 2; ++j){
-      int gc = bn + wc*32 + j*16 + id;
-      #pragma unroll
-      for (int rr = 0; rr < 4; ++rr){
-        int row = gr0 + rr;
-        if (row >= M) continue;
-        YB[(size_t)row*256 + gc] = f2h(acc1[i][j][rr]);
-        ZB[(size_t)row*256 + gc] = f2h(acc2[i][j][rr]);
-      }
-    }
-  }
-}
-
-__device__ __forceinline__ void gru_phase_ps(
-    const unsigned short* __restrict__ AH, const unsigned short* __restrict__ AL,
-    const unsigned short* __restrict__ WH_, const unsigned short* __restrict__ WL_,
-    int bm, int bn, int tid, int wr, int wc, int quad, int id,
-    unsigned short* AsH, unsigned short* AsL,
-    unsigned short* W0H, unsigned short* W0L,
-    unsigned short* W1H, unsigned short* W1L,
-    unsigned short* W2H, unsigned short* W2L,
-    f32x4 (&accR)[2][2], f32x4 (&accZ)[2][2], f32x4 (&accN)[2][2])
-{
-  for (int kt = 0; kt < 8; ++kt){
-    int k0 = kt * 32;
-    stagePS(AH, AL, 256, bm, k0, AsH, AsL, tid);
-    stagePS(WH_,          WL_,          256, bn, k0, W0H, W0L, tid);
-    stagePS(WH_ + 65536,  WL_ + 65536,  256, bn, k0, W1H, W1L, tid);
-    stagePS(WH_ + 131072, WL_ + 131072, 256, bn, k0, W2H, W2L, tid);
-    __syncthreads();
-    short8 aH[2], aL[2];
-    #pragma unroll
-    for (int i = 0; i < 2; ++i){
-      int off = ldsOff(wr*32 + i*16 + id, quad);
-      aH[i] = *(const short8*)&AsH[off];
-      aL[i] = *(const short8*)&AsL[off];
-    }
-    #pragma unroll
-    for (int j = 0; j < 2; ++j){
-      int off = ldsOff(wc*32 + j*16 + id, quad);
-      short8 bh, bl;
-      bh = *(const short8*)&W0H[off]; bl = *(const short8*)&W0L[off];
-      #pragma unroll
-      for (int i = 0; i < 2; ++i) accR[i][j] = mfma3(aH[i], aL[i], bh, bl, accR[i][j]);
-      bh = *(const short8*)&W1H[off]; bl = *(const short8*)&W1L[off];
-      #pragma unroll
-      for (int i = 0; i < 2; ++i) accZ[i][j] = mfma3(aH[i], aL[i], bh, bl, accZ[i][j]);
-      bh = *(const short8*)&W2H[off]; bl = *(const short8*)&W2L[off];
-      #pragma unroll
-      for (int i = 0; i < 2; ++i) accN[i][j] = mfma3(aH[i], aL[i], bh, bl, accN[i][j]);
-    }
-    __syncthreads();
-  }
-}
-
-__global__ __launch_bounds__(256) void gru_ps_k(
-    const unsigned short* __restrict__ XinH, const unsigned short* __restrict__ XinL,
-    const unsigned short* __restrict__ HidH, const unsigned short* __restrict__ HidL,
-    const unsigned short* __restrict__ wihH, const unsigned short* __restrict__ wihL,
-    const unsigned short* __restrict__ whhH, const unsigned short* __restrict__ whhL,
-    const float* __restrict__ bih, const float* __restrict__ bhh,
-    unsigned short* __restrict__ OutH, unsigned short* __restrict__ OutL, int M)
-{
-  __shared__ unsigned short AsH[64*32], AsL[64*32];
-  __shared__ unsigned short W0H[64*32], W0L[64*32];
-  __shared__ unsigned short W1H[64*32], W1L[64*32];
-  __shared__ unsigned short W2H[64*32], W2L[64*32];
-  int nwg = gridDim.x, bid = blockIdx.x;
-  int q = nwg >> 3, r = nwg & 7;
-  int xcd = bid & 7, jj = bid >> 3;
-  int idx = (xcd < r ? xcd*(q+1) : r*(q+1) + (xcd - r)*q) + jj;
-  const int bm = (idx >> 2)*64, bn = (idx & 3)*64;
-  const int tid = threadIdx.x;
-  const int wave = tid >> 6, lane = tid & 63;
-  const int wr = wave >> 1, wc = wave & 1;
-  const int quad = lane >> 4, id = lane & 15;
-
-  f32x4 accR[2][2] = {}, accZ[2][2] = {}, accI[2][2] = {}, accH[2][2] = {};
-
-  gru_phase_ps(XinH, XinL, wihH, wihL, bm, bn, tid, wr, wc, quad, id,
-               AsH, AsL, W0H, W0L, W1H, W1L, W2H, W2L, accR, accZ, accI);
-  gru_phase_ps(HidH, HidL, whhH, whhL, bm, bn, tid, wr, wc, quad, id,
-               AsH, AsL, W0H, W0L, W1H, W1L, W2H, W2L, accR, accZ, accH);
-
-  #pragma unroll
-  for (int i = 0; i < 2; ++i){
-    int gr0 = bm + wr*32 + i*16 + quad*4;
-    #pragma unroll
-    for (int j = 0; j < 2; ++j){
-      int gc = bn + wc*32 + j*16 + id;
-      float br_  = bih[gc]     + bhh[gc];
-      float bz_  = bih[256+gc] + bhh[256+gc];
-      float bn_i = bih[512+gc], bn_h = bhh[512+gc];
-      #pragma unroll
-      for (int rr = 0; rr < 4; ++rr){
-        int row = gr0 + rr;
-        if (row >= M) continue;
-        float rg = sigf(accR[i][j][rr] + br_);
-        float zg = sigf(accZ[i][j][rr] + bz_);
-        float ng = tanhf(accI[i][j][rr] + bn_i + rg*(accH[i][j][rr] + bn_h));
-        float hv = rec2(HidH[(size_t)row*256 + gc], HidL[(size_t)row*256 + gc]);
-        float o = (1.f - zg)*ng + zg*hv;
-        o = o > 0.f ? o : 0.f;
-        unsigned short h, l; split2(o, h, l);
-        OutH[(size_t)row*256 + gc] = h;
-        OutL[(size_t)row*256 + gc] = l;
-      }
-    }
-  }
-}
-
-__global__ __launch_bounds__(256) void rowdot2_ps_k(
-    const unsigned short* __restrict__ XH, const unsigned short* __restrict__ XL,
-    const float* __restrict__ w1, const float* __restrict__ w2,
-    float* __restrict__ y1, float* __restrict__ y2, int M)
-{
-  int m = blockIdx.x*4 + (threadIdx.x >> 6);
-  if (m >= M) return;
-  int lane = threadIdx.x & 63;
-  us4 vh = *(const us4*)&XH[(size_t)m*256 + lane*4];
-  us4 vl = *(const us4*)&XL[(size_t)m*256 + lane*4];
-  float p1 = 0.f, p2 = 0.f;
-  #pragma unroll
-  for (int u = 0; u < 4; ++u){
-    float xv = rec2(vh[u], vl[u]);
-    int c = lane*4 + u;
-    p1 += xv * w1[c];
-    if (w2) p2 += xv * w2[c];
-  }
-  for (int o = 32; o > 0; o >>= 1){
-    p1 += __shfl_down(p1, o);
-    if (w2) p2 += __shfl_down(p2, o);
-  }
-  if (lane == 0){ y1[m] = p1; if (w2) y2[m] = p2; }
-}
-
-__global__ __launch_bounds__(256) void rowdot_b_k(
+__global__ __launch_bounds__(256) void rowdot_h_k(
     const unsigned short* __restrict__ XB,
     const float* __restrict__ w1, const float* __restrict__ w2,
     float* __restrict__ y1, float* __restrict__ y2, int M)
@@ -620,7 +774,7 @@
     const unsigned short* __restrict__ ZB,
     const float* __restrict__ w, const unsigned* __restrict__ off,
     const int* __restrict__ csr_src, const float* __restrict__ bias,
-    unsigned short* __restrict__ hH, unsigned short* __restrict__ hL, int N)
+    unsigned short* __restrict__ hB, int N)
 {
   int n = blockIdx.x*4 + (threadIdx.x >> 6);
   if (n >= N) return;
@@ -644,20 +798,13 @@
     }
   }
   const float4 b = *(const float4*)&bias[lane*4];
-  float vals[4];
+  us4 vo;
   float v;
-  v = acc.x + b.x; vals[0] = v > 0.f ? v : expf(v) - 1.f;
-  v = acc.y + b.y; vals[1] = v > 0.f ? v : expf(v) - 1.f;
-  v = acc.z + b.z; vals[2] = v > 0.f ? v : expf(v) - 1.f;
-  v = acc.w + b.w; vals[3] = v > 0.f ? v : expf(v) - 1.f;
-  us4 vh, vl;
-  #pragma unroll
-  for (int u = 0; u < 4; ++u){
-    unsigned short h, l; split2(vals[u], h, l);
-    vh[u] = h; vl[u] = l;
-  }
-  *(us4*)&hH[(size_t)n*256 + lane*4] = vh;
-  *(us4*)&hL[(size_t)n*256 + lane*4] = vl;
+  v = acc.x + b.x; vo[0] = f2h(v > 0.f ? v : expf(v) - 1.f);
+  v = acc.y + b.y; vo[1] = f2h(v > 0.f ? v : expf(v) - 1.f);
+  v = acc.z + b.z; vo[2] = f2h(v > 0.f ? v : expf(v) - 1.f);
+  v = acc.w + b.w; vo[3] = f2h(v > 0.f ? v : expf(v) - 1.f);
+  *(us4*)&hB[(size_t)n*256 + lane*4] = vo;
 }
 
 __global__ void seg_bounds_k(const int* __restrict__ batch, unsigned* __restrict__ gs,
@@ -669,19 +816,19 @@
   atomicMax(&ge[g], (unsigned)(n+1));
 }
 __global__ __launch_bounds__(256) void graph_pool_k(
-    const unsigned short* __restrict__ xH, const unsigned short* __restrict__ xL,
+    const unsigned short* __restrict__ xB,
     const unsigned* __restrict__ gs, const unsigned* __restrict__ ge,
-    unsigned short* __restrict__ outgH, unsigned short* __restrict__ outgL)
+    unsigned short* __restrict__ ogH, unsigned short* __restrict__ ogL)
 {
   int g = blockIdx.x, t = threadIdx.x;
   unsigned s0 = gs[g], e0 = ge[g];
   float acc = 0.f;
   for (unsigned n = s0; n < e0; ++n)
-    acc += rec2(xH[(size_t)n*256 + t], xL[(size_t)n*256 + t]);
+    acc += h2f(xB[(size_t)n*256 + t]);
   acc = acc > 0.f ? acc : 0.f;
-  unsigned short h, l; split2(acc, h, l);
-  outgH[(size_t)g*256 + t] = h;
-  outgL[(size_t)g*256 + t] = l;
+  unsigned short h, l; split2h(acc, h, l);
+  ogH[(size_t)g*256 + t] = h;
+  ogL[(size_t)g*256 + t] = l;
 }
 __global__ void precompute_v_k(const float* __restrict__ W, const float* __restrict__ ad,
                                float* __restrict__ v){
@@ -700,7 +847,7 @@
 {
   __shared__ float red[256];
   int g = blockIdx.x, t = threadIdx.x;
-  float ogv = rec2(ogH[(size_t)g*256 + t], ogL[(size_t)g*256 + t]);
+  float ogv = rec2h(ogH[(size_t)g*256 + t], ogL[(size_t)g*256 + t]);
   float tg = blkSum(ogv * v[t], red);
   unsigned s0 = gs[g], e0 = geb[g];
   float mx = -INFINITY;
@@ -719,7 +866,7 @@
   }
   float h0 = acc + bias[t];
   h0 = h0 > 0.f ? h0 : expf(h0) - 1.f;
-  unsigned short h, l; split2(h0, h, l);
+  unsigned short h, l; split2h(h0, h, l);
   hgH[(size_t)g*256 + t] = h;
   hgL[(size_t)g*256 + t] = l;
 }
@@ -785,10 +932,10 @@
   };
   auto allocUS = [&](size_t elems)->unsigned short*{ return (unsigned short*)alloc(elems*2); };
 
-  unsigned short *xH   = allocUS((size_t)N*H), *xL   = allocUS((size_t)N*H);
-  unsigned short *hbH  = allocUS((size_t)N*H), *hbL  = allocUS((size_t)N*H);
-  unsigned short *outH = allocUS((size_t)N*H), *outL = allocUS((size_t)N*H);
-  unsigned short *xwB  = allocUS((size_t)N*H);
+  unsigned short *x   = allocUS((size_t)N*H);
+  unsigned short *hb  = allocUS((size_t)N*H);
+  unsigned short *out = allocUS((size_t)N*H);
+  unsigned short *xw  = allocUS((size_t)N*H);
   float*    ea    = (float*)alloc((size_t)E*4);
   float*    nd1   = (float*)alloc((size_t)N*4);
   float*    nd2   = (float*)alloc((size_t)N*4);
@@ -821,34 +968,27 @@
   unsigned short *gl1H  = allocUS(WS), *gl1L = allocUS(WS);
   unsigned short *gl2H  = allocUS(WS), *gl2L = allocUS(WS);
   unsigned short *atWH  = allocUS(WS*NL), *atWL = allocUS(WS*NL);
-  unsigned short *molH  = allocUS(WS), *molL = allocUS(WS);
+  unsigned short *molWH = allocUS(WS), *molWL = allocUS(WS);
   unsigned short *l2WH  = allocUS((size_t)NHID*256), *l2WL = allocUS((size_t)NHID*256);
   unsigned short *f1WH  = allocUS((size_t)NOUT*NHID), *f1WL = allocUS((size_t)NOUT*NHID);
 
-  auto gemmps = [&](const unsigned short* AH_, const unsigned short* AL_,
-                    const unsigned short* WH_, const unsigned short* WL_,
-                    const float* bias, float* C, unsigned short* CH, unsigned short* CL,
-                    int M_, int N_, int K_, int op){
-    int ncb = N_ / 64;
-    int nwg = ((M_ + 63)/64) * ncb;
-    gemm_ps_k<<<dim3(nwg), dim3(256), 0, stream>>>(AH_, AL_, WH_, WL_, bias, C, CH, CL,
-                                                   M_, N_, K_, op, ncb);
+  auto gemms = [&](const unsigned short* A_, const unsigned short* WH_,
+                   const unsigned short* WL_, unsigned short* CB, int M_){
+    int nwg = ((M_ + 63)/64)*4;
+    gemm16s_k<<<dim3(nwg), dim3(256), 0, stream>>>(A_, WH_, WL_, CB, M_);
   };
-  auto grup = [&](const unsigned short* XiH, const unsigned short* XiL,
-                  const unsigned short* HiH, const unsigned short* HiL,
+  auto gruN = [&](const unsigned short* Xi, const unsigned short* Hi,
                   const unsigned short* ihH, const unsigned short* ihL,
                   const unsigned short* hhH, const unsigned short* hhL,
                   const float* bih, const float* bhh,
-                  unsigned short* OH, unsigned short* OL, int M_){
+                  unsigned short* O, int M_){
     int nwg = ((M_ + 63)/64)*4;
-    gru_ps_k<<<dim3(nwg), dim3(256), 0, stream>>>(XiH, XiL, HiH, HiL,
-                                                  ihH, ihL, hhH, hhL, bih, bhh,
-                                                  OH, OL, M_);
+    gru16_k<<<dim3(nwg), dim3(256), 0, stream>>>(Xi, Hi, ihH, ihL, hhH, hhL, bih, bhh, O, M_);
   };
   auto wsplit = [&](const float* src, unsigned short* Hd, unsigned short* Ld,
                     int lda, int K, long long rows){
     long long tot = rows * K;
-    wsplit_k<<<dim3((unsigned)((tot + 255)/256)), dim3(256), 0, stream>>>(src, Hd, Ld, lda, K, tot);
+    wsplit16_k<<<dim3((unsigned)((tot + 255)/256)), dim3(256), 0, stream>>>(src, Hd, Ld, lda, K, tot);
   };
 
   wsplit(gru0_wih, g0ihH, g0ihL, 256, 256, 768);
@@ -860,9 +1000,9 @@
   wsplit(g_lin1W,  gl1H, gl1L, H+1, 256, 256);
   wsplit(g_lin2W,  gl2H, gl2L, 256, 256, 256);
   wsplit(atom_W,   atWH, atWL, 256, 256, (long long)NL*256);
-  wsplit(mol_W,    molH, molL, 256, 256, 256);
-  wsplit(lin2_W,   l2WH, l2WL, 256, 256, NHID);
-  wsplit(fc1_W,    f1WH, f1WL, NHID, NHID, NOUT);
+  wsplit(mol_W,    molWH, molWL, 256, 256, 256);
+  wsplit(lin2_W, l2WH, l2WL, 256, 256, NHID);
+  wsplit(fc1_W,  f1WH, f1WL, NHID, NHID, NOUT);
 
   hipMemsetAsync(deg, 0, (size_t)N*4, stream);
   hist_k<<<dim3((E+255)/256), dim3(256), 0, stream>>>(dstI, deg, E);
@@ -881,59 +1021,68 @@
 
   {
     dim3 gr(4, (N + 63)/64);
-    gemm_mfma_k<<<gr, dim3(256), 0, stream>>>(x_in, NIN, lin1_W, NIN, lin1_b,
-                                              xH, xL, N, H, NIN, OP_LRELU);
+    gemm_l1_k<<<gr, dim3(256), 0, stream>>>(x_in, NIN, lin1_W, NIN, lin1_b,
+                                            x, N, H, NIN, OP_LRELU);
   }
 
   {
     int nwg = ((N + 63)/64)*4;
-    gemm2_ps_k<<<dim3(nwg), dim3(256), 0, stream>>>(xH, xL, gl1H, gl1L, gl2H, gl2L,
-                                                    outH, xwB, N);
-  }
-  rowdot2_ps_k<<<dim3((N+3)/4), dim3(256), 0, stream>>>(xH, xL, g_att_r, (const float*)nullptr,
-                                                        nd1, (float*)nullptr, N);
-  gate_edge_score_csc_k<<<dim3((N+3)/4), dim3(256), 0, stream>>>(outH, g_lin1W, g_att_l,
+    gemm2s_k<<<dim3(nwg), dim3(256), 0, stream>>>(x, gl1H, gl1L, gl2H, gl2L, out, xw, N);
+  }
+  rowdot_h_k<<<dim3((N+3)/4), dim3(256), 0, stream>>>(x, g_att_r, (const float*)nullptr,
+                                                      nd1, (float*)nullptr, N);
+  gate_edge_score_csc_k<<<dim3((N+3)/4), dim3(256), 0, stream>>>(out, g_lin1W, g_att_l,
                                                                  ea_in, nd1, off2, csc_pos,
                                                                  csr_eid, dstI, ea, N, H);
   node_softmax_k<<<dim3(nb), dim3(256), 0, stream>>>(off, csr_src, nullptr, nullptr, ea, N, 0);
-  gather_h_k<<<dim3((N+3)/4), dim3(256), 0, stream>>>(xwB, ea, off, csr_src, g_bias,
-                                                      hbH, hbL, N);
-  grup(hbH, hbL, xH, xL, g0ihH, g0ihL, g0hhH, g0hhL, gru0_bih, gru0_bhh, outH, outL, N);
-  { unsigned short* t = xH; xH = outH; outH = t; t = xL; xL = outL; outL = t; }
+  gather_h_k<<<dim3((N+3)/4), dim3(256), 0, stream>>>(xw, ea, off, csr_src, g_bias, hb, N);
+  gruN(hb, x, g0ihH, g0ihL, g0hhH, g0hhL, gru0_bih, gru0_bhh, out, N);
+  { unsigned short* t = x; x = out; out = t; }
 
   for (int l = 0; l < NL; ++l){
-    gemmps(xH, xL, atWH + (size_t)l*WS, atWL + (size_t)l*WS, nullptr,
-           nullptr, xwB, nullptr, N, 256, 256, OP_NONE);
-    rowdot_b_k<<<dim3((N+3)/4), dim3(256), 0, stream>>>(xwB, atom_as + (size_t)l*H,
+    gemms(x, atWH + (size_t)l*WS, atWL + (size_t)l*WS, xw, N);
+    rowdot_h_k<<<dim3((N+3)/4), dim3(256), 0, stream>>>(xw, atom_as + (size_t)l*H,
                                                         atom_ad + (size_t)l*H, nd1, nd2, N);
     node_softmax_k<<<dim3(nb), dim3(256), 0, stream>>>(off, csr_src, nd1, nd2, ea, N, 1);
-    gather_h_k<<<dim3((N+3)/4), dim3(256), 0, stream>>>(xwB, ea, off, csr_src,
-                                                        atom_b + (size_t)l*H, hbH, hbL, N);
-    grup(hbH, hbL, xH, xL,
-         aihH + (size_t)l*WG, aihL + (size_t)l*WG,
+    gather_h_k<<<dim3((N+3)/4), dim3(256), 0, stream>>>(xw, ea, off, csr_src,
+                                                        atom_b + (size_t)l*H, hb, N);
+    gruN(hb, x, aihH + (size_t)l*WG, aihL + (size_t)l*WG,
          ahhH + (size_t)l*WG, ahhL + (size_t)l*WG,
-         agru_bih + (size_t)l*3*H, agru_bhh + (size_t)l*3*H, outH, outL, N);
-    { unsigned short* t = xH; xH = outH; outH = t; t = xL; xL = outL; outL = t; }
+         agru_bih + (size_t)l*3*H, agru_bhh + (size_t)l*3*H, out, N);
+    { unsigned short* t = x; x = out; out = t; }
   }
 
   hipMemsetAsync(gsb, 0xFF, (size_t)G*4, stream);
   hipMemsetAsync(geb, 0x00, (size_t)G*4, stream);
   seg_bounds_k<<<dim3((N+255)/256), dim3(256), 0, stream>>>(batch, gsb, geb, N);
-  graph_pool_k<<<dim3(G), dim3(256), 0, stream>>>(xH, xL, gsb, geb, ogH, ogL);
-  gemmps(xH, xL, molH, molL, nullptr, nullptr, xwB, nullptr, N, 256, 256, OP_NONE);
-  rowdot_b_k<<<dim3((N+3)/4), dim3(256), 0, stream>>>(xwB, mol_as, (const float*)nullptr,
+  graph_pool_k<<<dim3(G), dim3(256), 0, stream>>>(x, gsb, geb, ogH, ogL);
+  gemms(x, molWH, molWL, xw, N);
+  rowdot_h_k<<<dim3((N+3)/4), dim3(256), 0, stream>>>(xw, mol_as, (const float*)nullptr,
                                                       nd1, (float*)nullptr, N);
   precompute_v_k<<<dim3(1), dim3(256), 0, stream>>>(mol_W, mol_ad, vvec);
   unsigned short *cogH = ogH, *cogL = ogL, *cog2H = og2H, *cog2L = og2L;
   for (int t = 0; t < T; ++t){
-    mol_pool_k<<<dim3(G), dim3(256), 0, stream>>>(cogH, cogL, vvec, nd1, xwB,
+    mol_pool_k<<<dim3(G), dim3(256), 0, stream>>>(cogH, cogL, vvec, nd1, xw,
                                                   gsb, geb, mol_b, hgH, hgL);
-    grup(hgH, hgL, cogH, cogL, mihH, mihL, mhhH, mhhL, mgru_bih, mgru_bhh,
-         cog2H, cog2L, G);
+    gru16m_k<<<dim3(((G+63)/64)*4), dim3(256), 0, stream>>>(hgH, hgL, cogH, cogL,
+                                                            mihH, mihL, mhhH, mhhL,
+                                                            mgru_bih, mgru_bhh,
+                                                            cog2H, cog2L, G);
     { unsigned short* tt = cogH; cogH = cog2H; cog2H = tt;
       tt = cogL; cogL = cog2L; cog2L = tt; }
   }
 
-  gemmps(cogH, cogL, l2WH, l2WL, lin2_b, nullptr, o2H, o2L, G, NHID, 256, OP_RELU);
-  gemmps(o2H, o2L, f1WH, f1WL, fc1_b, (float*)d_out, nullptr, nullptr, G, NOUT, NHID, OP_NONE);
-}
+  {
+    int ncb = NHID / 64;
+    int nwg = ((G + 63)/64) * ncb;
+    gemm16p_k<<<dim3(nwg), dim3(256), 0, stream>>>(cogH, cogL, l2WH, l2WL, lin2_b,
+                                                   nullptr, o2H, o2L, G, NHID, 256, OP_RELU, ncb);
+  }
+  {
+    int ncb = NOUT / 64;
+    int nwg = ((G + 63)/64) * ncb;
+    gemm16p_k<<<dim3(nwg), dim3(256), 0, stream>>>(o2H, o2L, f1WH, f1WL, fc1_b,
+                                                   (float*)d_out, nullptr, nullptr,
+                                                   G, NOUT, NHID, OP_NONE, ncb);
+  }
+}
```

New measurement: 3.210 ms. -12.2%, faster.
